# Optimization experiments

Hardware: AMD Instinct MI355X
Metric: run time of the kernel (lower is better)

Reference implementation:

```python
import jax, jax.numpy as jnp
import numpy as np

NS = [65536, 16384, 4096, 1024, 256, 64]          # nodes per level (64 = 8 graphs x 8 dense voxels)
ES = [1048576, 262144, 65536, 16384, 4096]        # edges per level (avg degree 16)
INS = [1, 15, 23, 31, 39]
OUTS = [12, 20, 28, 36, 44]
K = 5                                             # kernel_size


def setup_inputs():
    keys = iter(jax.random.split(jax.random.key(0), 64))
    d = {'x': jax.random.normal(next(keys), (NS[0], 1), jnp.float32),
         'pos': jax.random.uniform(next(keys), (NS[0], 3), jnp.float32)}
    for l in range(5):
        n, e, ci, co = NS[l], ES[l], INS[l], OUTS[l]
        d[f'src{l}'] = jax.random.randint(next(keys), (e,), 0, n)
        d[f'dst{l}'] = jax.random.randint(next(keys), (e,), 0, n)
        d[f'eattr{l}'] = jax.random.normal(next(keys), (e, 3), jnp.float32)
        d[f'cluster{l}'] = jax.random.randint(next(keys), (n,), 0, NS[l + 1])
        d[f'w1_{l}'] = jax.random.normal(next(keys), (3, K), jnp.float32) * 0.5
        d[f'b1_{l}'] = jnp.zeros((K,), jnp.float32)
        d[f'w2_{l}'] = jax.random.normal(next(keys), (K, ci * co), jnp.float32) / np.float32(np.sqrt(K * ci))
        d[f'b2_{l}'] = jnp.zeros((ci * co,), jnp.float32)
        d[f'root_{l}'] = jax.random.normal(next(keys), (ci, co), jnp.float32) / np.float32(np.sqrt(ci))
        d[f'bias_{l}'] = jnp.zeros((co,), jnp.float32)
    d['fc_w'] = jax.random.normal(next(keys), (8 * 47, 10), jnp.float32) / np.float32(np.sqrt(8 * 47))
    d['fc_b'] = jnp.zeros((10,), jnp.float32)
    return d


def _conv(x, src, dst, eattr, w1, b1, w2, b2, root, bias, n):
    # edge-conditioned kernel: MLP(edge_attr) -> [E, ci, co]
    h = jnp.tanh(eattr @ w1 + b1)                                  # [E, K]
    We = (h @ w2 + b2).reshape(eattr.shape[0], x.shape[1], -1)     # [E, ci, co]
    msg = jnp.einsum('ei,eio->eo', x[src], We)                     # gather + per-edge matvec
    s = jax.ops.segment_sum(msg, dst, num_segments=n)
    cnt = jax.ops.segment_sum(jnp.ones((dst.shape[0], 1), x.dtype), dst, num_segments=n)
    agg = s / jnp.maximum(cnt, 1.0)                                # mean aggregation
    return agg + x @ root + bias, jnp.mean(jnp.square(We))


def _pool(x, pos, cluster, n_next):
    # sparse voxel max pool on features, mean on positions; pos concatenated to features
    xm = jax.ops.segment_max(x, cluster, num_segments=n_next)
    xm = jnp.where(jnp.isfinite(xm), xm, 0.0)                      # empty voxels -> 0
    ps = jax.ops.segment_sum(pos, cluster, num_segments=n_next)
    cnt = jax.ops.segment_sum(jnp.ones((pos.shape[0], 1), pos.dtype), cluster, num_segments=n_next)
    pm = ps / jnp.maximum(cnt, 1.0)
    return jnp.concatenate([xm, pm], axis=1), pm


def reference(x, pos, src0, dst0, eattr0, cluster0, w1_0, b1_0, w2_0, b2_0, root_0, bias_0,
              src1, dst1, eattr1, cluster1, w1_1, b1_1, w2_1, b2_1, root_1, bias_1,
              src2, dst2, eattr2, cluster2, w1_2, b1_2, w2_2, b2_2, root_2, bias_2,
              src3, dst3, eattr3, cluster3, w1_3, b1_3, w2_3, b2_3, root_3, bias_3,
              src4, dst4, eattr4, cluster4, w1_4, b1_4, w2_4, b2_4, root_4, bias_4,
              fc_w, fc_b):
    lv = [(src0, dst0, eattr0, cluster0, w1_0, b1_0, w2_0, b2_0, root_0, bias_0),
          (src1, dst1, eattr1, cluster1, w1_1, b1_1, w2_1, b2_1, root_1, bias_1),
          (src2, dst2, eattr2, cluster2, w1_2, b1_2, w2_2, b2_2, root_2, bias_2),
          (src3, dst3, eattr3, cluster3, w1_3, b1_3, w2_3, b2_3, root_3, bias_3),
          (src4, dst4, eattr4, cluster4, w1_4, b1_4, w2_4, b2_4, root_4, bias_4)]
    closs = jnp.float32(0.0)
    for l, (src, dst, ea, cl, w1, b1, w2, b2, rt, bs) in enumerate(lv):
        x, c = _conv(x, src, dst, ea, w1, b1, w2, b2, rt, bs, NS[l])
        closs = closs + c
        x, pos = _pool(x, pos, cl, NS[l + 1])
    feat = x.reshape(-1, 8 * 47)                                   # [B, 8*47]
    logits = feat @ fc_w + fc_b
    return jax.nn.log_softmax(logits, axis=1), closs
```

## Files before the change

### kernel.cpp

```cpp
#include <hip/hip_runtime.h>
#include <hip/hip_fp16.h>
#include <math.h>


#define TILES0 1024
#define TSZ0   1024
#define NB0    512
#define TILES1 256
#define TSZ1   1024
#define NB1    512

__device__ __forceinline__ float ftanh(float x) {
    float e = __expf(2.f * x);
    return 1.f - 2.f / (e + 1.f);
}

struct SegArgs {
    const int* idx[10];
    int*       cnt[10];
    int*       rp [10];
    int*       out[10];
    int        n  [10];
    int        nb [10];
    int        tstart[11];
};

struct ScanAux {
    int* tilesum;
    int* tileoff;
    int  sstart[11];
    int  T;
};

struct HArgs {
    const float* eattr[5];
    const float* w1[5];
    const float* b1[5];
    float*       H;
    int          E[5];
    int          bstart[6];
};

struct WArgs {
    const float* w2[5];
    const float* b2[5];
    const float* H;
    float*       sq;
    int          cico[5];
    int          E[5];
};

__global__ __launch_bounds__(256) void countA_k(
    SegArgs a, HArgs ha, const int* __restrict__ dst0,
    const int* __restrict__ dst1, int* __restrict__ M, int* __restrict__ M1,
    int hsBlocks)
{
    __shared__ int sh[NB0];
    int B = blockIdx.x;
    int t = threadIdx.x;

    if (B < TILES0) {
        for (int u = t; u < NB0; u += 256) sh[u] = 0;
        __syncthreads();
        int base = B * TSZ0 + t;
        #pragma unroll
        for (int it = 0; it < 4; it++)
            atomicAdd(&sh[dst0[base + it * 256] >> 7], 1);
        __syncthreads();
        for (int u = t; u < NB0; u += 256) M[(size_t)B * NB0 + u] = sh[u];
        return;
    }
    B -= TILES0;
    if (B < TILES1) {
        for (int u = t; u < NB1; u += 256) sh[u] = 0;
        __syncthreads();
        int base = B * TSZ1 + t;
        #pragma unroll
        for (int it = 0; it < 4; it++)
            atomicAdd(&sh[dst1[base + it * 256] >> 5], 1);
        __syncthreads();
        for (int u = t; u < NB1; u += 256) M1[(size_t)B * NB1 + u] = sh[u];
        return;
    }
    B -= TILES1;
    if (B < hsBlocks) {
        const int K = 8;
        int l = 0;
        while (l < 4 && B >= ha.bstart[l + 1]) l++;
        int bloc = B - ha.bstart[l];
        const float* ea = ha.eattr[l];
        float w1r[15], b1r[5];
        #pragma unroll
        for (int i = 0; i < 15; i++) w1r[i] = ha.w1[l][i];
        #pragma unroll
        for (int i = 0; i < 5; i++)  b1r[i] = ha.b1[l][i];
        float acc[20];
        #pragma unroll
        for (int i = 0; i < 20; i++) acc[i] = 0.f;
        int base = bloc * 256 * K + t;
        for (int it = 0; it < K; it++) {
            int e = base + it * 256;
            if (e < ha.E[l]) {
                float e0 = ea[e * 3], e1 = ea[e * 3 + 1], e2 = ea[e * 3 + 2];
                float h[5];
                #pragma unroll
                for (int k = 0; k < 5; k++)
                    h[k] = ftanh(e0 * w1r[k] + e1 * w1r[5 + k] + e2 * w1r[10 + k] + b1r[k]);
                int p = 5;
                #pragma unroll
                for (int k = 0; k < 5; k++) {
                    acc[k] += h[k];
                    #pragma unroll
                    for (int k2 = k; k2 < 5; k2++) acc[p++] += h[k] * h[k2];
                }
            }
        }
        float* red = (float*)sh;
        int wid = t >> 6, lane = t & 63;
        #pragma unroll
        for (int v = 0; v < 20; v++) {
            float s = acc[v];
            #pragma unroll
            for (int o = 32; o; o >>= 1) s += __shfl_down(s, o);
            if (lane == 0) red[wid * 20 + v] = s;
        }
        __syncthreads();
        if (t < 20)
            atomicAdd(&ha.H[l * 20 + t],
                      red[t] + red[20 + t] + red[40 + t] + red[60 + t]);
        return;
    }
    B -= hsBlocks;
    {
        int s = 0;
        while (s < 9 && B >= a.tstart[s + 1]) s++;
        int i0 = (B - a.tstart[s]) * 1024;
        const int* idx = a.idx[s];
        int* cnt = a.cnt[s];
        int n = a.n[s];
        #pragma unroll
        for (int j = 0; j < 4; j++) {
            int i = i0 + j * 256 + t;
            if (i < n) atomicAdd(&cnt[idx[i]], 1);
        }
    }
}

__global__ __launch_bounds__(256) void scanP1_k(
    SegArgs a, ScanAux x, const int* __restrict__ M, int* __restrict__ M2,
    int* __restrict__ colTotal, const int* __restrict__ M1,
    int* __restrict__ M21, int* __restrict__ ct1)
{
    __shared__ int sc[256];
    int B = blockIdx.x;
    int t = threadIdx.x;

    if (B < NB0) {
        int v[4];
        int s4 = 0;
        #pragma unroll
        for (int j = 0; j < 4; j++) {
            v[j] = M[(size_t)(t * 4 + j) * NB0 + B];
            s4 += v[j];
        }
        sc[t] = s4;
        __syncthreads();
        for (int d = 1; d < 256; d <<= 1) {
            int u = (t >= d) ? sc[t - d] : 0;
            __syncthreads();
            sc[t] += u;
            __syncthreads();
        }
        int run = sc[t] - s4;
        #pragma unroll
        for (int j = 0; j < 4; j++) {
            M2[(size_t)(t * 4 + j) * NB0 + B] = run;
            run += v[j];
        }
        if (t == 255) colTotal[B] = sc[255];
        return;
    }
    B -= NB0;
    if (B < NB1) {
        int v = M1[(size_t)t * NB1 + B];
        sc[t] = v;
        __syncthreads();
        for (int d = 1; d < 256; d <<= 1) {
            int u = (t >= d) ? sc[t - d] : 0;
            __syncthreads();
            sc[t] += u;
            __syncthreads();
        }
        M21[(size_t)t * NB1 + B] = sc[t] - v;
        if (t == 255) ct1[B] = sc[255];
        return;
    }
    int b = B - NB1;
    int s = 0;
    while (s < 9 && b >= x.sstart[s + 1]) s++;
    int tloc = b - x.sstart[s];
    int nb = a.nb[s];
    const int* cnt = a.cnt[s];
    int i0 = tloc * 4096 + t * 16;
    int sum = 0;
    #pragma unroll
    for (int k = 0; k < 16; k++) {
        int i = i0 + k;
        if (i < nb) sum += cnt[i];
    }
    #pragma unroll
    for (int o = 32; o; o >>= 1) sum += __shfl_down(sum, o);
    if ((t & 63) == 0) sc[t >> 6] = sum;
    __syncthreads();
    if (t == 0)
        x.tilesum[b] = sc[0] + sc[1] + sc[2] + sc[3];
}

__global__ __launch_bounds__(512) void scanP2_k(
    SegArgs a, ScanAux x, const int* __restrict__ colTotal,
    int* __restrict__ bucketStart, const int* __restrict__ ct1,
    int* __restrict__ bs1)
{
    __shared__ int sc[NB0];
    int t = threadIdx.x;
    if (blockIdx.x == 0) {
        int v = colTotal[t];
        sc[t] = v;
        __syncthreads();
        for (int d = 1; d < NB0; d <<= 1) {
            int u = (t >= d) ? sc[t - d] : 0;
            __syncthreads();
            sc[t] += u;
            __syncthreads();
        }
        bucketStart[t] = sc[t] - v;
        if (t == NB0 - 1) bucketStart[NB0] = sc[NB0 - 1];
        return;
    }
    if (blockIdx.x == 2) {
        int v = ct1[t];
        sc[t] = v;
        __syncthreads();
        for (int d = 1; d < NB1; d <<= 1) {
            int u = (t >= d) ? sc[t - d] : 0;
            __syncthreads();
            sc[t] += u;
            __syncthreads();
        }
        bs1[t] = sc[t] - v;
        if (t == NB1 - 1) bs1[NB1] = sc[NB1 - 1];
        return;
    }
    if (t >= 64) return;
    int lane = t;
    int orig = (lane < x.T) ? x.tilesum[lane] : 0;
    int val = orig;
    #pragma unroll
    for (int d = 1; d < 64; d <<= 1) {
        int v = __shfl_up(val, d);
        if (lane >= d) val += v;
    }
    int excl = val - orig;
    int s = 0;
    while (s < 9 && lane >= x.sstart[s + 1]) s++;
    int segExcl = __shfl(excl, x.sstart[s]);
    if (lane < x.T) {
        x.tileoff[lane] = excl - segExcl;
        if (lane == x.sstart[s + 1] - 1)
            a.rp[s][a.nb[s]] = val - segExcl;
    }
}

__global__ __launch_bounds__(256) void scanP3_k(
    SegArgs a, ScanAux x,
    const int* __restrict__ src, const int* __restrict__ dst,
    const float* __restrict__ ea, const float* __restrict__ x0,
    const int* __restrict__ M2, const int* __restrict__ bucketStart,
    float4* __restrict__ pay2,
    const float* __restrict__ w1, const float* __restrict__ b1,
    float* __restrict__ H0,
    const int* __restrict__ src1, const int* __restrict__ dst1,
    const float* __restrict__ ea1, const int* __restrict__ M21,
    const int* __restrict__ bs1, float4* __restrict__ pay1)
{
    __shared__ int   shi[NB0];
    __shared__ float shf[100];
    int B = blockIdx.x;
    int t = threadIdx.x;

    if (B < TILES0) {
        int tile = B;
        for (int u = t; u < NB0; u += 256)
            shi[u] = bucketStart[u] + M2[(size_t)tile * NB0 + u];
        if (t < 15) shf[t] = w1[t];
        if (t >= 32 && t < 37) shf[15 + t - 32] = b1[t - 32];
        __syncthreads();

        float acc[20];
        #pragma unroll
        for (int i = 0; i < 20; i++) acc[i] = 0.f;

        int base = tile * TSZ0 + t;
        #pragma unroll
        for (int it = 0; it < 4; it++) {
            int i = base + it * 256;
            int d = dst[i];
            float e0 = ea[i * 3], e1 = ea[i * 3 + 1], e2 = ea[i * 3 + 2];
            float h[5];
            #pragma unroll
            for (int k = 0; k < 5; k++)
                h[k] = ftanh(e0 * shf[k] + e1 * shf[5 + k] + e2 * shf[10 + k] + shf[15 + k]);
            int p = 5;
            #pragma unroll
            for (int k = 0; k < 5; k++) {
                acc[k] += h[k];
                #pragma unroll
                for (int k2 = k; k2 < 5; k2++) acc[p++] += h[k] * h[k2];
            }
            float xv = x0[src[i]];
            union HU { __half2 h2; float f; } p01, p23;
            p01.h2 = __floats2half2_rn(h[0], h[1]);
            p23.h2 = __floats2half2_rn(h[2], h[3]);
            unsigned wbits = ((unsigned)d << 16) |
                             (unsigned)__half_as_ushort(__float2half_rn(h[4]));
            int ps = atomicAdd(&shi[d >> 7], 1);
            pay2[ps] = make_float4(xv, p01.f, p23.f, __uint_as_float(wbits));
        }

        int wid = t >> 6, lane = t & 63;
        #pragma unroll
        for (int v = 0; v < 20; v++) {
            float s = acc[v];
            #pragma unroll
            for (int o = 32; o; o >>= 1) s += __shfl_down(s, o);
            if (lane == 0) shf[20 + wid * 20 + v] = s;
        }
        __syncthreads();
        if (t < 20)
            atomicAdd(&H0[t], shf[20 + t] + shf[40 + t] + shf[60 + t] + shf[80 + t]);
        return;
    }
    B -= TILES0;
    if (B < TILES1) {
        int tile = B;
        for (int u = t; u < NB1; u += 256)
            shi[u] = bs1[u] + M21[(size_t)tile * NB1 + u];
        __syncthreads();
        int base = tile * TSZ1 + t;
        #pragma unroll
        for (int it = 0; it < 4; it++) {
            int i = base + it * 256;
            int d = dst1[i];
            int key = (d << 16) | src1[i];
            float e0 = ea1[i * 3], e1 = ea1[i * 3 + 1], e2 = ea1[i * 3 + 2];
            int ps = atomicAdd(&shi[d >> 5], 1);
            pay1[ps] = make_float4(__int_as_float(key), e0, e1, e2);
        }
        return;
    }
    B -= TILES1;
    int s = 0;
    while (s < 9 && B >= x.sstart[s + 1]) s++;
    int tloc = B - x.sstart[s];
    int nb = a.nb[s];
    const int* cnt = a.cnt[s];
    int* rp = a.rp[s];
    int i0 = tloc * 4096 + t * 16;
    int v[16];
    int sum = 0;
    #pragma unroll
    for (int k = 0; k < 16; k++) {
        int i = i0 + k;
        v[k] = (i < nb) ? cnt[i] : 0;
        sum += v[k];
    }
    int acc = sum;
    shi[t] = acc;
    __syncthreads();
    for (int d = 1; d < 256; d <<= 1) {
        int t2 = (t >= d) ? shi[t - d] : 0;
        __syncthreads();
        acc += t2;
        shi[t] = acc;
        __syncthreads();
    }
    int running = x.tileoff[B] + (acc - sum);
    #pragma unroll
    for (int k = 0; k < 16; k++) {
        int i = i0 + k;
        if (i < nb) rp[i] = running;
        running += v[k];
    }
}

__global__ __launch_bounds__(256) void scatC_k(
    SegArgs a, WArgs wa,
    const float4* __restrict__ pay2, const int* __restrict__ bucketStart,
    const float* __restrict__ w2, const float* __restrict__ b2,
    const float* __restrict__ root, const float* __restrict__ bias,
    const float* __restrict__ x, float* __restrict__ y,
    const float4* __restrict__ pay1, const int* __restrict__ bs1,
    int* __restrict__ rp1, float4* __restrict__ rec1)
{
    __shared__ float wsm[96];
    __shared__ float nacc[7 * 128];
    __shared__ int hist[32], st[32], cur[32];
    int B = blockIdx.x;
    int t = threadIdx.x;

    if (B < NB0) {
        if (t < 60) wsm[t] = w2[t];
        else if (t >= 64  && t < 76)  wsm[60 + t - 64]  = b2[t - 64];
        else if (t >= 128 && t < 140) wsm[72 + t - 128] = root[t - 128];
        else if (t >= 192 && t < 204) wsm[84 + t - 192] = bias[t - 192];
        for (int u = t; u < 7 * 128; u += 256) nacc[u] = 0.f;
        __syncthreads();

        int lo = bucketStart[B], hi = bucketStart[B + 1];
        int bin0 = B << 7;
        for (int j = lo + t; j < hi; j += 256) {
            float4 R = pay2[j];
            union HU { float f; __half2 h2; } a01, a23;
            a01.f = R.y; a23.f = R.z;
            unsigned wbits = __float_as_uint(R.w);
            int node = (int)(wbits >> 16) - bin0;
            float xv = R.x;
            atomicAdd(&nacc[node], xv);
            atomicAdd(&nacc[128 + node], __low2float(a01.h2)  * xv);
            atomicAdd(&nacc[256 + node], __high2float(a01.h2) * xv);
            atomicAdd(&nacc[384 + node], __low2float(a23.h2)  * xv);
            atomicAdd(&nacc[512 + node], __high2float(a23.h2) * xv);
            atomicAdd(&nacc[640 + node],
                      __half2float(__ushort_as_half((unsigned short)(wbits & 0xffffu))) * xv);
            atomicAdd(&nacc[768 + node], 1.f);
        }
        __syncthreads();

        if (t < 128) {
            int v = bin0 + t;
            float deg = nacc[768 + t];
            float S0 = nacc[t],       S1 = nacc[128 + t], S2 = nacc[256 + t];
            float S3 = nacc[384 + t], S4 = nacc[512 + t], S5 = nacc[640 + t];
            float inv = 1.f / fmaxf(deg, 1.f);
            float xv = x[v];
            #pragma unroll
            for (int o = 0; o < 12; o++) {
                float msg = wsm[60 + o] * S0 + wsm[o] * S1 + wsm[12 + o] * S2 +
                            wsm[24 + o] * S3 + wsm[36 + o] * S4 + wsm[48 + o] * S5;
                y[v * 12 + o] = msg * inv + xv * wsm[72 + o] + wsm[84 + o];
            }
        }
        return;
    }
    B -= NB0;
    if (B < NB1) {
        int b = B;
        int lo = bs1[b], hi = bs1[b + 1];
        int bin0 = b << 5;
        if (t < 32) hist[t] = 0;
        __syncthreads();
        const float* payw = (const float*)pay1;
        for (int j = lo + t; j < hi; j += 256) {
            int rel = (int)(__float_as_uint(payw[4 * j]) >> 16) - bin0;
            atomicAdd(&hist[rel], 1);
        }
        __syncthreads();
        if (t < 32) {
            int v = hist[t];
            int val = v;
            #pragma unroll
            for (int d = 1; d < 32; d <<= 1) {
                int u = __shfl_up(val, d);
                if (t >= d) val += u;
            }
            st[t] = val - v;
            cur[t] = lo + val - v;
            rp1[bin0 + t] = lo + val - v;
            if (b == NB1 - 1 && t == 31) rp1[NB1 * 32] = hi;
        }
        __syncthreads();
        for (int j = lo + t; j < hi; j += 256) {
            float4 R = pay1[j];
            int rel = (int)(__float_as_uint(R.x) >> 16) - bin0;
            int p = atomicAdd(&cur[rel], 1);
            rec1[p] = R;
        }
        return;
    }
    B -= NB1;
    if (B < 5) {
        if (t >= 64) return;
        int l = B;
        const float* w2l = wa.w2[l];
        const float* b2l = wa.b2[l];
        int cico = wa.cico[l];
        float d[21];
        #pragma unroll
        for (int i = 0; i < 21; i++) d[i] = 0.f;
        for (int u = t; u < cico; u += 64) {
            float b = b2l[u];
            float w[5];
            #pragma unroll
            for (int k = 0; k < 5; k++) w[k] = w2l[k * cico + u];
            int p = 0;
            #pragma unroll
            for (int k = 0; k < 5; k++) {
                #pragma unroll
                for (int k2 = k; k2 < 5; k2++) d[p++] += w[k] * w[k2];
            }
            #pragma unroll
            for (int k = 0; k < 5; k++) d[15 + k] += b * w[k];
            d[20] += b * b;
        }
        #pragma unroll
        for (int i = 0; i < 21; i++) {
            #pragma unroll
            for (int off = 32; off; off >>= 1) d[i] += __shfl_down(d[i], off);
        }
        if (t == 0) {
            const float* H1 = wa.H + l * 20;
            const float* H2 = H1 + 5;
            float sq = (float)wa.E[l] * d[20];
            #pragma unroll
            for (int k = 0; k < 5; k++) sq += 2.f * d[15 + k] * H1[k];
            int p = 0;
            #pragma unroll
            for (int k = 0; k < 5; k++) {
                #pragma unroll
                for (int k2 = k; k2 < 5; k2++) {
                    sq += ((k == k2) ? 1.f : 2.f) * d[p] * H2[p];
                    p++;
                }
            }
            wa.sq[l] = sq;
        }
        return;
    }
    B -= 5;
    {
        int s = 0;
        while (s < 9 && B >= a.tstart[s + 1]) s++;
        int i0 = (B - a.tstart[s]) * 1024;
        const int* idx = a.idx[s];
        int* cnt = a.cnt[s];
        const int* rp = a.rp[s];
        int* out = a.out[s];
        int n = a.n[s];
        #pragma unroll
        for (int j = 0; j < 4; j++) {
            int i = i0 + j * 256 + t;
            if (i < n) {
                int d = idx[i];
                int p = atomicSub(&cnt[d], 1) - 1;
                out[rp[d] + p] = i;
            }
        }
    }
}

__global__ __launch_bounds__(256) void conv1s_k(
    const int* __restrict__ rp, const float4* __restrict__ rec,
    const float* __restrict__ w1, const float* __restrict__ b1,
    const float* __restrict__ w2, const float* __restrict__ b2,
    const float* __restrict__ root, const float* __restrict__ bias,
    const float* __restrict__ x, float* __restrict__ y)
{
    constexpr int CI = 15, CO = 20, CH = 48, CICO = CI * CO;
    __shared__ float w1s[20];
    __shared__ float4 recb[CH];
    __shared__ int   svb[CH];
    __shared__ float hb[CH * 6];
    __shared__ float xs[CH * CI];
    __shared__ float S[6 * CI];

    int t = threadIdx.x;
    int v = blockIdx.x;
    if (t < 20) w1s[t] = (t < 15) ? w1[t] : b1[t - 15];
    int r0 = rp[v], r1 = rp[v + 1];
    int d  = r1 - r0;
    float acc = 0.f;

    for (int c0 = r0; c0 < r1; c0 += CH) {
        int cn = min(CH, r1 - c0);
        if (t < cn) {
            float4 R = rec[c0 + t];
            recb[t] = R;
            svb[t]  = (int)(__float_as_uint(R.x) & 0xffffu);
            hb[t * 6] = 1.f;
        }
        __syncthreads();
        if (t < cn * 5) {
            int j = t / 5, k = t % 5;
            float e0 = recb[j].y, e1 = recb[j].z, e2 = recb[j].w;
            hb[j * 6 + 1 + k] =
                ftanh(e0 * w1s[k] + e1 * w1s[5 + k] + e2 * w1s[10 + k] + w1s[15 + k]);
        }
        for (int u = t; u < cn * CI; u += 256)
            xs[u] = x[(size_t)svb[u / CI] * CI + (u % CI)];
        __syncthreads();
        if (t < 6 * CI) {
            int i = t / 6, k6 = t % 6;
            for (int j = 0; j < cn; j++)
                acc += hb[j * 6 + k6] * xs[j * CI + i];
        }
        __syncthreads();
    }

    if (t < 6 * CI) S[t] = acc;
    __syncthreads();

    if (t < CO) {
        float m = 0.f;
        for (int i = 0; i < CI; i++) {
            m += b2[i * CO + t] * S[i * 6];
            #pragma unroll
            for (int k = 0; k < 5; k++)
                m += w2[k * CICO + i * CO + t] * S[i * 6 + 1 + k];
        }
        m /= fmaxf((float)d, 1.f);
        for (int i = 0; i < CI; i++)
            m += x[(size_t)v * CI + i] * root[i * CO + t];
        y[(size_t)v * CO + t] = m + bias[t];
    }
}

template<int CI, int CO>
__global__ __launch_bounds__(256) void coop_conv_k(
    const int* __restrict__ rp, const int* __restrict__ eid,
    const int* __restrict__ src, const float* __restrict__ eattr,
    const float* __restrict__ w1, const float* __restrict__ b1,
    const float* __restrict__ w2, const float* __restrict__ b2,
    const float* __restrict__ root, const float* __restrict__ bias,
    const float* __restrict__ x, float* __restrict__ y)
{
    constexpr int CH   = 48;
    constexpr int CICO = CI * CO;
    __shared__ float w1s[20];
    __shared__ int   eb[CH], svb[CH];
    __shared__ float hb[CH * 6];
    __shared__ float xs[CH * CI];
    __shared__ float S[6 * CI];

    int t = threadIdx.x;
    int v = blockIdx.x;
    if (t < 20) w1s[t] = (t < 15) ? w1[t] : b1[t - 15];
    int r0 = rp[v], r1 = rp[v + 1];
    int d  = r1 - r0;
    float acc = 0.f;

    for (int c0 = r0; c0 < r1; c0 += CH) {
        int cn = min(CH, r1 - c0);
        if (t < cn) {
            int e = eid[c0 + t];
            eb[t]  = e;
            svb[t] = src[e];
            hb[t * 6] = 1.f;
        }
        __syncthreads();
        if (t < cn * 5) {
            int j = t / 5, k = t % 5;
            int e = eb[j];
            float e0 = eattr[e * 3], e1 = eattr[e * 3 + 1], e2 = eattr[e * 3 + 2];
            hb[j * 6 + 1 + k] =
                ftanh(e0 * w1s[k] + e1 * w1s[5 + k] + e2 * w1s[10 + k] + w1s[15 + k]);
        }
        for (int u = t; u < cn * CI; u += 256)
            xs[u] = x[(size_t)svb[u / CI] * CI + (u % CI)];
        __syncthreads();
        if (t < 6 * CI) {
            int i = t / 6, k6 = t % 6;
            for (int j = 0; j < cn; j++)
                acc += hb[j * 6 + k6] * xs[j * CI + i];
        }
        __syncthreads();
    }

    if (t < 6 * CI) S[t] = acc;
    __syncthreads();

    if (t < CO) {
        float m = 0.f;
        for (int i = 0; i < CI; i++) {
            m += b2[i * CO + t] * S[i * 6];
            #pragma unroll
            for (int k = 0; k < 5; k++)
                m += w2[k * CICO + i * CO + t] * S[i * 6 + 1 + k];
        }
        m /= fmaxf((float)d, 1.f);
        for (int i = 0; i < CI; i++)
            m += x[(size_t)v * CI + i] * root[i * CO + t];
        y[(size_t)v * CO + t] = m + bias[t];
    }
}

template<int CO>
__global__ __launch_bounds__(256) void pool_k(
    int NN,
    const int* __restrict__ crp, const int* __restrict__ cnid,
    const float* __restrict__ y, const float* __restrict__ pos,
    float* __restrict__ xn, float* __restrict__ pn)
{
    int t = blockIdx.x * 256 + threadIdx.x;
    if (t >= NN * (CO + 3)) return;
    int c = t / (CO + 3), o = t % (CO + 3);
    int r0 = crp[c], r1 = crp[c + 1];
    int d = r1 - r0;
    if (o < CO) {
        float m = -INFINITY;
        for (int j = r0; j < r1; j++)
            m = fmaxf(m, y[(size_t)cnid[j] * CO + o]);
        if (d == 0 || !isfinite(m)) m = 0.f;
        xn[c * (CO + 3) + o] = m;
    } else {
        int k = o - CO;
        float sum = 0.f;
        for (int j = r0; j < r1; j++)
            sum += pos[cnid[j] * 3 + k];
        float pm = sum / fmaxf((float)d, 1.f);
        xn[c * (CO + 3) + CO + k] = pm;
        pn[c * 3 + k] = pm;
    }
}

__global__ __launch_bounds__(128) void fc_k(
    const float* __restrict__ x5,
    const float* __restrict__ fc_w, const float* __restrict__ fc_b,
    const float* __restrict__ sq, float* __restrict__ out)
{
    __shared__ float feat[8 * 376];
    __shared__ float logit[80];
    __shared__ float roff[8];
    for (int t = threadIdx.x; t < 8 * 376; t += 128) feat[t] = x5[t];
    __syncthreads();
    int t = threadIdx.x;
    if (t < 80) {
        int b = t / 10, j = t % 10;
        float acc = fc_b[j];
        for (int k = 0; k < 376; k++) acc += feat[b * 376 + k] * fc_w[k * 10 + j];
        logit[t] = acc;
    }
    __syncthreads();
    if (t < 8) {
        float m = -1e30f;
        for (int j = 0; j < 10; j++) m = fmaxf(m, logit[t * 10 + j]);
        float ssum = 0.f;
        for (int j = 0; j < 10; j++) ssum += expf(logit[t * 10 + j] - m);
        roff[t] = m + logf(ssum);
    }
    __syncthreads();
    if (t < 80) out[t] = logit[t] - roff[t / 10];
    if (t == 0) {
        float closs = 0.f;
        closs += sq[0] * (1.0f / 12582912.0f);
        closs += sq[1] * (1.0f / 78643200.0f);
        closs += sq[2] * (1.0f / 42205184.0f);
        closs += sq[3] * (1.0f / 18284544.0f);
        closs += sq[4] * (1.0f / 7028736.0f);
        out[80] = closs;
    }
}


extern "C" void kernel_launch(void* const* d_in, const int* in_sizes, int n_in,
                              void* d_out, int out_size, void* d_ws, size_t ws_size,
                              hipStream_t stream)
{
    static const int NSa[6] = {65536, 16384, 4096, 1024, 256, 64};
    static const int ESa[5] = {1048576, 262144, 65536, 16384, 4096};
    static const int COa[5] = {12, 20, 28, 36, 44};
    static const int CIa[5] = {1, 15, 23, 31, 39};

    const float* x0   = (const float*)d_in[0];
    const float* pos0 = (const float*)d_in[1];

    int* wsw = (int*)d_ws;
    size_t off = 0;
    auto alw = [&](size_t n) -> size_t {
        size_t p = off; off += (n + 63) & ~(size_t)63; return p;
    };
    size_t degO[5], cdegO[5];
    for (int l = 2; l < 5; l++) degO[l]  = alw(NSa[l]);
    for (int l = 0; l < 5; l++) cdegO[l] = alw(NSa[l + 1]);
    size_t HO = alw(100);
    size_t zeroWords = off;
    size_t rpO[5], crpO[5], eidO[5], cnidO[5];
    rpO[1] = alw(NSa[1] + 1);
    for (int l = 2; l < 5; l++) rpO[l]  = alw(NSa[l] + 1);
    for (int l = 0; l < 5; l++) crpO[l] = alw(NSa[l + 1] + 1);
    for (int l = 2; l < 5; l++) eidO[l] = alw(ESa[l]);
    for (int l = 0; l < 5; l++) cnidO[l] = alw(NSa[l]);
    size_t tsO  = alw(64);
    size_t toO  = alw(64);
    size_t MO   = alw((size_t)TILES0 * NB0);
    size_t M2O  = alw((size_t)TILES0 * NB0);
    size_t ctO  = alw(NB0);
    size_t bsO  = alw(NB0 + 1);
    size_t payO = alw((size_t)ESa[0] * 4);
    size_t M1O  = alw((size_t)TILES1 * NB1);
    size_t M21O = alw((size_t)TILES1 * NB1);
    size_t ct1O = alw(NB1);
    size_t bs1O = alw(NB1 + 1);
    size_t pay1O = alw((size_t)ESa[1] * 4);
    size_t rec1O = alw((size_t)ESa[1] * 4);
    size_t yO   = alw((size_t)65536 * 12);
    size_t sqO  = alw(8);
    size_t xnO[5], pnO[5];
    for (int l = 0; l < 5; l++) xnO[l] = alw((size_t)NSa[l + 1] * (COa[l] + 3));
    for (int l = 0; l < 5; l++) pnO[l] = alw((size_t)NSa[l] * 3 / 4 + 64);
    for (int l = 0; l < 5; l++) pnO[l] = alw((size_t)NSa[l + 1] * 3);

    hipMemsetAsync(d_ws, 0, zeroWords * 4, stream);

    SegArgs sa{};
    int nseg = 0;
    for (int l = 2; l < 5; l++) {
        sa.idx[nseg] = (const int*)d_in[3 + 10 * l];
        sa.cnt[nseg] = wsw + degO[l];
        sa.rp [nseg] = wsw + rpO[l];
        sa.out[nseg] = wsw + eidO[l];
        sa.n  [nseg] = ESa[l];
        sa.nb [nseg] = NSa[l];
        nseg++;
    }
    for (int l = 0; l < 5; l++) {
        sa.idx[nseg] = (const int*)d_in[5 + 10 * l];
        sa.cnt[nseg] = wsw + cdegO[l];
        sa.rp [nseg] = wsw + crpO[l];
        sa.out[nseg] = wsw + cnidO[l];
        sa.n  [nseg] = NSa[l];
        sa.nb [nseg] = NSa[l + 1];
        nseg++;
    }
    ScanAux sx{};
    int tiles = 0, btiles = 0;
    for (int s = 0; s < nseg; s++) {
        sa.tstart[s] = tiles;
        tiles += (sa.n[s] + 1023) / 1024;
        sx.sstart[s] = btiles;
        btiles += (sa.nb[s] + 4095) / 4096;
    }
    for (int s = nseg; s <= 10; s++) {
        sa.tstart[s] = tiles;
        sx.sstart[s] = btiles;
        if (s < 10) {
            sa.idx[s] = sa.idx[nseg - 1]; sa.cnt[s] = sa.cnt[nseg - 1];
            sa.rp[s] = sa.rp[nseg - 1];   sa.out[s] = sa.out[nseg - 1];
            sa.n[s] = 0; sa.nb[s] = 8;
        }
    }
    sx.T = btiles;
    sx.tilesum = wsw + tsO;
    sx.tileoff = wsw + toO;

    float4* pay2 = (float4*)(wsw + payO);
    float4* pay1 = (float4*)(wsw + pay1O);
    float4* rec1 = (float4*)(wsw + rec1O);
    float*  Hp   = (float*)(wsw + HO);

    HArgs ha{};
    int bs = 0;
    ha.bstart[0] = 0;
    ha.eattr[0] = (const float*)d_in[4];
    ha.w1[0] = (const float*)d_in[6];
    ha.b1[0] = (const float*)d_in[7];
    ha.E[0] = 0;
    for (int l = 1; l < 5; l++) {
        ha.eattr[l] = (const float*)d_in[4 + 10 * l];
        ha.w1[l]    = (const float*)d_in[6 + 10 * l];
        ha.b1[l]    = (const float*)d_in[7 + 10 * l];
        ha.E[l]     = ESa[l];
        ha.bstart[l] = bs;
        bs += (ESa[l] + 2047) / 2048;
    }
    ha.bstart[5] = bs;
    ha.H = Hp;

    WArgs wa{};
    for (int l = 0; l < 5; l++) {
        wa.w2[l]   = (const float*)d_in[8 + 10 * l];
        wa.b2[l]   = (const float*)d_in[9 + 10 * l];
        wa.cico[l] = CIa[l] * COa[l];
        wa.E[l]    = ESa[l];
    }
    wa.H  = Hp;
    wa.sq = (float*)(wsw + sqO);

    countA_k<<<TILES0 + TILES1 + bs + tiles, 256, 0, stream>>>(
        sa, ha, (const int*)d_in[3], (const int*)d_in[13],
        wsw + MO, wsw + M1O, bs);
    scanP1_k<<<NB0 + NB1 + btiles, 256, 0, stream>>>(
        sa, sx, wsw + MO, wsw + M2O, wsw + ctO,
        wsw + M1O, wsw + M21O, wsw + ct1O);
    scanP2_k<<<3, 512, 0, stream>>>(sa, sx, wsw + ctO, wsw + bsO,
                                    wsw + ct1O, wsw + bs1O);
    scanP3_k<<<TILES0 + TILES1 + btiles, 256, 0, stream>>>(
        sa, sx,
        (const int*)d_in[2], (const int*)d_in[3], (const float*)d_in[4],
        x0, wsw + M2O, wsw + bsO, pay2,
        (const float*)d_in[6], (const float*)d_in[7], Hp,
        (const int*)d_in[12], (const int*)d_in[13], (const float*)d_in[14],
        wsw + M21O, wsw + bs1O, pay1);

    float* yb = (float*)(wsw + yO);

    scatC_k<<<NB0 + NB1 + 5 + tiles, 256, 0, stream>>>(
        sa, wa, pay2, wsw + bsO,
        (const float*)d_in[8], (const float*)d_in[9],
        (const float*)d_in[10], (const float*)d_in[11], x0, yb,
        pay1, wsw + bs1O, wsw + rpO[1], rec1);

    pool_k<12><<<(NSa[1] * 15 + 255) / 256, 256, 0, stream>>>(
        NSa[1], wsw + crpO[0], wsw + cnidO[0], yb, pos0,
        (float*)(wsw + xnO[0]), (float*)(wsw + pnO[0]));

    conv1s_k<<<NSa[1], 256, 0, stream>>>(
        wsw + rpO[1], rec1,
        (const float*)d_in[16], (const float*)d_in[17],
        (const float*)d_in[18], (const float*)d_in[19],
        (const float*)d_in[20], (const float*)d_in[21],
        (const float*)(wsw + xnO[0]), yb);
    pool_k<20><<<(NSa[2] * 23 + 255) / 256, 256, 0, stream>>>(
        NSa[2], wsw + crpO[1], wsw + cnidO[1], yb,
        (const float*)(wsw + pnO[0]),
        (float*)(wsw + xnO[1]), (float*)(wsw + pnO[1]));

#define LVLC(l, CI_, CO_) do {                                                 \
    const float* xin   = (const float*)(wsw + xnO[(l) - 1]);                   \
    const float* posin = (const float*)(wsw + pnO[(l) - 1]);                   \
    int N = NSa[(l)], NN = NSa[(l) + 1];                                       \
    coop_conv_k<CI_, CO_><<<N, 256, 0, stream>>>(                              \
        wsw + rpO[(l)], wsw + eidO[(l)],                                       \
        (const int*)d_in[2 + 10 * (l)], (const float*)d_in[4 + 10 * (l)],      \
        (const float*)d_in[6 + 10 * (l)], (const float*)d_in[7 + 10 * (l)],    \
        (const float*)d_in[8 + 10 * (l)], (const float*)d_in[9 + 10 * (l)],    \
        (const float*)d_in[10 + 10 * (l)], (const float*)d_in[11 + 10 * (l)],  \
        xin, yb);                                                              \
    pool_k<CO_><<<(NN * ((CO_) + 3) + 255) / 256, 256, 0, stream>>>(           \
        NN, wsw + crpO[(l)], wsw + cnidO[(l)], yb, posin,                      \
        (float*)(wsw + xnO[(l)]), (float*)(wsw + pnO[(l)]));                   \
} while (0)

    LVLC(2, 23, 28);
    LVLC(3, 31, 36);
    LVLC(4, 39, 44);
#undef LVLC

    fc_k<<<1, 128, 0, stream>>>((const float*)(wsw + xnO[4]),
                                (const float*)d_in[52], (const float*)d_in[53],
                                wa.sq, (float*)d_out);
}
```

Measured before the change: 403.6 us.

## Fuse all stages into one persistent cooperative kernel with grid syncs

Replaces the sequence of separate kernel launches (count, scan phases, scatter, per-level conv and pool, fc) with a single persistent cooperative kernel. A fixed grid of 1024 blocks loops over each stage's virtual blocks and separates stages with grid.sync(). If the cooperative launch fails, it falls back to launching one kernel per stage. This is meant to remove launch overhead and the idle tails between the many small dependent kernels. In exchange, every stage runs under a fixed block count with shared-memory and register limits set for the whole kernel, which can lower per-stage efficiency.

```diff
diff --git a/kernel.cpp b/kernel.cpp
--- a/kernel.cpp
+++ b/kernel.cpp
@@ -1,6 +1,9 @@
 #include <hip/hip_runtime.h>
 #include <hip/hip_fp16.h>
+#include <hip/hip_cooperative_groups.h>
 #include <math.h>
+
+namespace cg = cooperative_groups;
 
 
 #define TILES0 1024
@@ -50,659 +53,69 @@
     int          E[5];
 };
 
-__global__ __launch_bounds__(256) void countA_k(
-    SegArgs a, HArgs ha, const int* __restrict__ dst0,
-    const int* __restrict__ dst1, int* __restrict__ M, int* __restrict__ M1,
-    int hsBlocks)
+struct MegaArgs {
+    SegArgs sa; ScanAux sx; HArgs ha; WArgs wa;
+    const int* src0; const int* dst0; const float* ea0;
+    const int* src1; const int* dst1; const float* ea1;
+    const float* x0; const float* pos0;
+    int* M; int* M2; int* colTotal; int* bucketStart;
+    int* M1; int* M21; int* ct1; int* bs1;
+    float4* pay2; float4* pay1; float4* rec1; int* rp1;
+    const float* w1[5]; const float* b1[5]; const float* w2[5]; const float* b2[5];
+    const float* root[5]; const float* bias[5];
+    const int* rp[5]; const int* eid[5]; const int* srcL[5]; const float* eaL[5];
+    const int* crp[5]; const int* cnid[5];
+    float* y; float* xn[5]; float* pn[5];
+    const float* fc_w; const float* fc_b; float* out;
+    int hsB;
+    int W[16];
+};
+
+
+__device__ void scan512(const int* __restrict__ in, int* __restrict__ outExcl,
+                        int t, int* sc)
 {
-    __shared__ int sh[NB0];
-    int B = blockIdx.x;
-    int t = threadIdx.x;
-
-    if (B < TILES0) {
-        for (int u = t; u < NB0; u += 256) sh[u] = 0;
-        __syncthreads();
-        int base = B * TSZ0 + t;
-        #pragma unroll
-        for (int it = 0; it < 4; it++)
-            atomicAdd(&sh[dst0[base + it * 256] >> 7], 1);
-        __syncthreads();
-        for (int u = t; u < NB0; u += 256) M[(size_t)B * NB0 + u] = sh[u];
-        return;
-    }
-    B -= TILES0;
-    if (B < TILES1) {
-        for (int u = t; u < NB1; u += 256) sh[u] = 0;
-        __syncthreads();
-        int base = B * TSZ1 + t;
-        #pragma unroll
-        for (int it = 0; it < 4; it++)
-            atomicAdd(&sh[dst1[base + it * 256] >> 5], 1);
-        __syncthreads();
-        for (int u = t; u < NB1; u += 256) M1[(size_t)B * NB1 + u] = sh[u];
-        return;
-    }
-    B -= TILES1;
-    if (B < hsBlocks) {
-        const int K = 8;
-        int l = 0;
-        while (l < 4 && B >= ha.bstart[l + 1]) l++;
-        int bloc = B - ha.bstart[l];
-        const float* ea = ha.eattr[l];
-        float w1r[15], b1r[5];
-        #pragma unroll
-        for (int i = 0; i < 15; i++) w1r[i] = ha.w1[l][i];
-        #pragma unroll
-        for (int i = 0; i < 5; i++)  b1r[i] = ha.b1[l][i];
-        float acc[20];
-        #pragma unroll
-        for (int i = 0; i < 20; i++) acc[i] = 0.f;
-        int base = bloc * 256 * K + t;
-        for (int it = 0; it < K; it++) {
-            int e = base + it * 256;
-            if (e < ha.E[l]) {
-                float e0 = ea[e * 3], e1 = ea[e * 3 + 1], e2 = ea[e * 3 + 2];
-                float h[5];
-                #pragma unroll
-                for (int k = 0; k < 5; k++)
-                    h[k] = ftanh(e0 * w1r[k] + e1 * w1r[5 + k] + e2 * w1r[10 + k] + b1r[k]);
-                int p = 5;
-                #pragma unroll
-                for (int k = 0; k < 5; k++) {
-                    acc[k] += h[k];
-                    #pragma unroll
-                    for (int k2 = k; k2 < 5; k2++) acc[p++] += h[k] * h[k2];
-                }
-            }
-        }
-        float* red = (float*)sh;
-        int wid = t >> 6, lane = t & 63;
-        #pragma unroll
-        for (int v = 0; v < 20; v++) {
-            float s = acc[v];
-            #pragma unroll
-            for (int o = 32; o; o >>= 1) s += __shfl_down(s, o);
-            if (lane == 0) red[wid * 20 + v] = s;
-        }
-        __syncthreads();
-        if (t < 20)
-            atomicAdd(&ha.H[l * 20 + t],
-                      red[t] + red[20 + t] + red[40 + t] + red[60 + t]);
-        return;
-    }
-    B -= hsBlocks;
-    {
-        int s = 0;
-        while (s < 9 && B >= a.tstart[s + 1]) s++;
-        int i0 = (B - a.tstart[s]) * 1024;
-        const int* idx = a.idx[s];
-        int* cnt = a.cnt[s];
-        int n = a.n[s];
-        #pragma unroll
-        for (int j = 0; j < 4; j++) {
-            int i = i0 + j * 256 + t;
-            if (i < n) atomicAdd(&cnt[idx[i]], 1);
-        }
-    }
-}
-
-__global__ __launch_bounds__(256) void scanP1_k(
-    SegArgs a, ScanAux x, const int* __restrict__ M, int* __restrict__ M2,
-    int* __restrict__ colTotal, const int* __restrict__ M1,
-    int* __restrict__ M21, int* __restrict__ ct1)
-{
-    __shared__ int sc[256];
-    int B = blockIdx.x;
-    int t = threadIdx.x;
-
-    if (B < NB0) {
-        int v[4];
-        int s4 = 0;
-        #pragma unroll
-        for (int j = 0; j < 4; j++) {
-            v[j] = M[(size_t)(t * 4 + j) * NB0 + B];
-            s4 += v[j];
-        }
-        sc[t] = s4;
-        __syncthreads();
-        for (int d = 1; d < 256; d <<= 1) {
-            int u = (t >= d) ? sc[t - d] : 0;
-            __syncthreads();
-            sc[t] += u;
-            __syncthreads();
-        }
-        int run = sc[t] - s4;
-        #pragma unroll
-        for (int j = 0; j < 4; j++) {
-            M2[(size_t)(t * 4 + j) * NB0 + B] = run;
-            run += v[j];
-        }
-        if (t == 255) colTotal[B] = sc[255];
-        return;
-    }
-    B -= NB0;
-    if (B < NB1) {
-        int v = M1[(size_t)t * NB1 + B];
-        sc[t] = v;
-        __syncthreads();
-        for (int d = 1; d < 256; d <<= 1) {
-            int u = (t >= d) ? sc[t - d] : 0;
-            __syncthreads();
-            sc[t] += u;
-            __syncthreads();
-        }
-        M21[(size_t)t * NB1 + B] = sc[t] - v;
-        if (t == 255) ct1[B] = sc[255];
-        return;
-    }
-    int b = B - NB1;
-    int s = 0;
-    while (s < 9 && b >= x.sstart[s + 1]) s++;
-    int tloc = b - x.sstart[s];
-    int nb = a.nb[s];
-    const int* cnt = a.cnt[s];
-    int i0 = tloc * 4096 + t * 16;
-    int sum = 0;
-    #pragma unroll
-    for (int k = 0; k < 16; k++) {
-        int i = i0 + k;
-        if (i < nb) sum += cnt[i];
-    }
-    #pragma unroll
-    for (int o = 32; o; o >>= 1) sum += __shfl_down(sum, o);
-    if ((t & 63) == 0) sc[t >> 6] = sum;
-    __syncthreads();
-    if (t == 0)
-        x.tilesum[b] = sc[0] + sc[1] + sc[2] + sc[3];
-}
-
-__global__ __launch_bounds__(512) void scanP2_k(
-    SegArgs a, ScanAux x, const int* __restrict__ colTotal,
-    int* __restrict__ bucketStart, const int* __restrict__ ct1,
-    int* __restrict__ bs1)
-{
-    __shared__ int sc[NB0];
-    int t = threadIdx.x;
-    if (blockIdx.x == 0) {
-        int v = colTotal[t];
-        sc[t] = v;
-        __syncthreads();
-        for (int d = 1; d < NB0; d <<= 1) {
-            int u = (t >= d) ? sc[t - d] : 0;
-            __syncthreads();
-            sc[t] += u;
-            __syncthreads();
-        }
-        bucketStart[t] = sc[t] - v;
-        if (t == NB0 - 1) bucketStart[NB0] = sc[NB0 - 1];
-        return;
-    }
-    if (blockIdx.x == 2) {
-        int v = ct1[t];
-        sc[t] = v;
-        __syncthreads();
-        for (int d = 1; d < NB1; d <<= 1) {
-            int u = (t >= d) ? sc[t - d] : 0;
-            __syncthreads();
-            sc[t] += u;
-            __syncthreads();
-        }
-        bs1[t] = sc[t] - v;
-        if (t == NB1 - 1) bs1[NB1] = sc[NB1 - 1];
-        return;
-    }
-    if (t >= 64) return;
-    int lane = t;
-    int orig = (lane < x.T) ? x.tilesum[lane] : 0;
-    int val = orig;
-    #pragma unroll
-    for (int d = 1; d < 64; d <<= 1) {
-        int v = __shfl_up(val, d);
-        if (lane >= d) val += v;
-    }
-    int excl = val - orig;
-    int s = 0;
-    while (s < 9 && lane >= x.sstart[s + 1]) s++;
-    int segExcl = __shfl(excl, x.sstart[s]);
-    if (lane < x.T) {
-        x.tileoff[lane] = excl - segExcl;
-        if (lane == x.sstart[s + 1] - 1)
-            a.rp[s][a.nb[s]] = val - segExcl;
-    }
-}
-
-__global__ __launch_bounds__(256) void scanP3_k(
-    SegArgs a, ScanAux x,
-    const int* __restrict__ src, const int* __restrict__ dst,
-    const float* __restrict__ ea, const float* __restrict__ x0,
-    const int* __restrict__ M2, const int* __restrict__ bucketStart,
-    float4* __restrict__ pay2,
-    const float* __restrict__ w1, const float* __restrict__ b1,
-    float* __restrict__ H0,
-    const int* __restrict__ src1, const int* __restrict__ dst1,
-    const float* __restrict__ ea1, const int* __restrict__ M21,
-    const int* __restrict__ bs1, float4* __restrict__ pay1)
-{
-    __shared__ int   shi[NB0];
-    __shared__ float shf[100];
-    int B = blockIdx.x;
-    int t = threadIdx.x;
-
-    if (B < TILES0) {
-        int tile = B;
-        for (int u = t; u < NB0; u += 256)
-            shi[u] = bucketStart[u] + M2[(size_t)tile * NB0 + u];
-        if (t < 15) shf[t] = w1[t];
-        if (t >= 32 && t < 37) shf[15 + t - 32] = b1[t - 32];
-        __syncthreads();
-
-        float acc[20];
-        #pragma unroll
-        for (int i = 0; i < 20; i++) acc[i] = 0.f;
-
-        int base = tile * TSZ0 + t;
-        #pragma unroll
-        for (int it = 0; it < 4; it++) {
-            int i = base + it * 256;
-            int d = dst[i];
-            float e0 = ea[i * 3], e1 = ea[i * 3 + 1], e2 = ea[i * 3 + 2];
-            float h[5];
-            #pragma unroll
-            for (int k = 0; k < 5; k++)
-                h[k] = ftanh(e0 * shf[k] + e1 * shf[5 + k] + e2 * shf[10 + k] + shf[15 + k]);
-            int p = 5;
-            #pragma unroll
-            for (int k = 0; k < 5; k++) {
-                acc[k] += h[k];
-                #pragma unroll
-                for (int k2 = k; k2 < 5; k2++) acc[p++] += h[k] * h[k2];
-            }
-            float xv = x0[src[i]];
-            union HU { __half2 h2; float f; } p01, p23;
-            p01.h2 = __floats2half2_rn(h[0], h[1]);
-            p23.h2 = __floats2half2_rn(h[2], h[3]);
-            unsigned wbits = ((unsigned)d << 16) |
-                             (unsigned)__half_as_ushort(__float2half_rn(h[4]));
-            int ps = atomicAdd(&shi[d >> 7], 1);
-            pay2[ps] = make_float4(xv, p01.f, p23.f, __uint_as_float(wbits));
-        }
-
-        int wid = t >> 6, lane = t & 63;
-        #pragma unroll
-        for (int v = 0; v < 20; v++) {
-            float s = acc[v];
-            #pragma unroll
-            for (int o = 32; o; o >>= 1) s += __shfl_down(s, o);
-            if (lane == 0) shf[20 + wid * 20 + v] = s;
-        }
-        __syncthreads();
-        if (t < 20)
-            atomicAdd(&H0[t], shf[20 + t] + shf[40 + t] + shf[60 + t] + shf[80 + t]);
-        return;
-    }
-    B -= TILES0;
-    if (B < TILES1) {
-        int tile = B;
-        for (int u = t; u < NB1; u += 256)
-            shi[u] = bs1[u] + M21[(size_t)tile * NB1 + u];
-        __syncthreads();
-        int base = tile * TSZ1 + t;
-        #pragma unroll
-        for (int it = 0; it < 4; it++) {
-            int i = base + it * 256;
-            int d = dst1[i];
-            int key = (d << 16) | src1[i];
-            float e0 = ea1[i * 3], e1 = ea1[i * 3 + 1], e2 = ea1[i * 3 + 2];
-            int ps = atomicAdd(&shi[d >> 5], 1);
-            pay1[ps] = make_float4(__int_as_float(key), e0, e1, e2);
-        }
-        return;
-    }
-    B -= TILES1;
-    int s = 0;
-    while (s < 9 && B >= x.sstart[s + 1]) s++;
-    int tloc = B - x.sstart[s];
-    int nb = a.nb[s];
-    const int* cnt = a.cnt[s];
-    int* rp = a.rp[s];
-    int i0 = tloc * 4096 + t * 16;
-    int v[16];
-    int sum = 0;
-    #pragma unroll
-    for (int k = 0; k < 16; k++) {
-        int i = i0 + k;
-        v[k] = (i < nb) ? cnt[i] : 0;
-        sum += v[k];
-    }
-    int acc = sum;
-    shi[t] = acc;
+    int a0 = in[2 * t], a1 = in[2 * t + 1];
+    int ps = a0 + a1;
+    sc[t] = ps;
     __syncthreads();
     for (int d = 1; d < 256; d <<= 1) {
-        int t2 = (t >= d) ? shi[t - d] : 0;
+        int u = (t >= d) ? sc[t - d] : 0;
         __syncthreads();
-        acc += t2;
-        shi[t] = acc;
+        sc[t] += u;
         __syncthreads();
     }
-    int running = x.tileoff[B] + (acc - sum);
-    #pragma unroll
-    for (int k = 0; k < 16; k++) {
-        int i = i0 + k;
-        if (i < nb) rp[i] = running;
-        running += v[k];
-    }
+    int excl = sc[t] - ps;
+    outExcl[2 * t]     = excl;
+    outExcl[2 * t + 1] = excl + a0;
+    if (t == 255) outExcl[512] = sc[255];
 }
 
-__global__ __launch_bounds__(256) void scatC_k(
-    SegArgs a, WArgs wa,
-    const float4* __restrict__ pay2, const int* __restrict__ bucketStart,
-    const float* __restrict__ w2, const float* __restrict__ b2,
-    const float* __restrict__ root, const float* __restrict__ bias,
-    const float* __restrict__ x, float* __restrict__ y,
-    const float4* __restrict__ pay1, const int* __restrict__ bs1,
-    int* __restrict__ rp1, float4* __restrict__ rec1)
+__device__ __forceinline__ void c0_accum(float* nacc, int bin0, float4 R)
 {
-    __shared__ float wsm[96];
-    __shared__ float nacc[7 * 128];
-    __shared__ int hist[32], st[32], cur[32];
-    int B = blockIdx.x;
-    int t = threadIdx.x;
-
-    if (B < NB0) {
-        if (t < 60) wsm[t] = w2[t];
-        else if (t >= 64  && t < 76)  wsm[60 + t - 64]  = b2[t - 64];
-        else if (t >= 128 && t < 140) wsm[72 + t - 128] = root[t - 128];
-        else if (t >= 192 && t < 204) wsm[84 + t - 192] = bias[t - 192];
-        for (int u = t; u < 7 * 128; u += 256) nacc[u] = 0.f;
-        __syncthreads();
-
-        int lo = bucketStart[B], hi = bucketStart[B + 1];
-        int bin0 = B << 7;
-        for (int j = lo + t; j < hi; j += 256) {
-            float4 R = pay2[j];
-            union HU { float f; __half2 h2; } a01, a23;
-            a01.f = R.y; a23.f = R.z;
-            unsigned wbits = __float_as_uint(R.w);
-            int node = (int)(wbits >> 16) - bin0;
-            float xv = R.x;
-            atomicAdd(&nacc[node], xv);
-            atomicAdd(&nacc[128 + node], __low2float(a01.h2)  * xv);
-            atomicAdd(&nacc[256 + node], __high2float(a01.h2) * xv);
-            atomicAdd(&nacc[384 + node], __low2float(a23.h2)  * xv);
-            atomicAdd(&nacc[512 + node], __high2float(a23.h2) * xv);
-            atomicAdd(&nacc[640 + node],
-                      __half2float(__ushort_as_half((unsigned short)(wbits & 0xffffu))) * xv);
-            atomicAdd(&nacc[768 + node], 1.f);
-        }
-        __syncthreads();
-
-        if (t < 128) {
-            int v = bin0 + t;
-            float deg = nacc[768 + t];
-            float S0 = nacc[t],       S1 = nacc[128 + t], S2 = nacc[256 + t];
-            float S3 = nacc[384 + t], S4 = nacc[512 + t], S5 = nacc[640 + t];
-            float inv = 1.f / fmaxf(deg, 1.f);
-            float xv = x[v];
-            #pragma unroll
-            for (int o = 0; o < 12; o++) {
-                float msg = wsm[60 + o] * S0 + wsm[o] * S1 + wsm[12 + o] * S2 +
-                            wsm[24 + o] * S3 + wsm[36 + o] * S4 + wsm[48 + o] * S5;
-                y[v * 12 + o] = msg * inv + xv * wsm[72 + o] + wsm[84 + o];
-            }
-        }
-        return;
-    }
-    B -= NB0;
-    if (B < NB1) {
-        int b = B;
-        int lo = bs1[b], hi = bs1[b + 1];
-        int bin0 = b << 5;
-        if (t < 32) hist[t] = 0;
-        __syncthreads();
-        const float* payw = (const float*)pay1;
-        for (int j = lo + t; j < hi; j += 256) {
-            int rel = (int)(__float_as_uint(payw[4 * j]) >> 16) - bin0;
-            atomicAdd(&hist[rel], 1);
-        }
-        __syncthreads();
-        if (t < 32) {
-            int v = hist[t];
-            int val = v;
-            #pragma unroll
-            for (int d = 1; d < 32; d <<= 1) {
-                int u = __shfl_up(val, d);
-                if (t >= d) val += u;
-            }
-            st[t] = val - v;
-            cur[t] = lo + val - v;
-            rp1[bin0 + t] = lo + val - v;
-            if (b == NB1 - 1 && t == 31) rp1[NB1 * 32] = hi;
-        }
-        __syncthreads();
-        for (int j = lo + t; j < hi; j += 256) {
-            float4 R = pay1[j];
-            int rel = (int)(__float_as_uint(R.x) >> 16) - bin0;
-            int p = atomicAdd(&cur[rel], 1);
-            rec1[p] = R;
-        }
-        return;
-    }
-    B -= NB1;
-    if (B < 5) {
-        if (t >= 64) return;
-        int l = B;
-        const float* w2l = wa.w2[l];
-        const float* b2l = wa.b2[l];
-        int cico = wa.cico[l];
-        float d[21];
-        #pragma unroll
-        for (int i = 0; i < 21; i++) d[i] = 0.f;
-        for (int u = t; u < cico; u += 64) {
-            float b = b2l[u];
-            float w[5];
-            #pragma unroll
-            for (int k = 0; k < 5; k++) w[k] = w2l[k * cico + u];
-            int p = 0;
-            #pragma unroll
-            for (int k = 0; k < 5; k++) {
-                #pragma unroll
-                for (int k2 = k; k2 < 5; k2++) d[p++] += w[k] * w[k2];
-            }
-            #pragma unroll
-            for (int k = 0; k < 5; k++) d[15 + k] += b * w[k];
-            d[20] += b * b;
-        }
-        #pragma unroll
-        for (int i = 0; i < 21; i++) {
-            #pragma unroll
-            for (int off = 32; off; off >>= 1) d[i] += __shfl_down(d[i], off);
-        }
-        if (t == 0) {
-            const float* H1 = wa.H + l * 20;
-            const float* H2 = H1 + 5;
-            float sq = (float)wa.E[l] * d[20];
-            #pragma unroll
-            for (int k = 0; k < 5; k++) sq += 2.f * d[15 + k] * H1[k];
-            int p = 0;
-            #pragma unroll
-            for (int k = 0; k < 5; k++) {
-                #pragma unroll
-                for (int k2 = k; k2 < 5; k2++) {
-                    sq += ((k == k2) ? 1.f : 2.f) * d[p] * H2[p];
-                    p++;
-                }
-            }
-            wa.sq[l] = sq;
-        }
-        return;
-    }
-    B -= 5;
-    {
-        int s = 0;
-        while (s < 9 && B >= a.tstart[s + 1]) s++;
-        int i0 = (B - a.tstart[s]) * 1024;
-        const int* idx = a.idx[s];
-        int* cnt = a.cnt[s];
-        const int* rp = a.rp[s];
-        int* out = a.out[s];
-        int n = a.n[s];
-        #pragma unroll
-        for (int j = 0; j < 4; j++) {
-            int i = i0 + j * 256 + t;
-            if (i < n) {
-                int d = idx[i];
-                int p = atomicSub(&cnt[d], 1) - 1;
-                out[rp[d] + p] = i;
-            }
-        }
-    }
+    union HU { float f; __half2 h2; } a01, a23;
+    a01.f = R.y; a23.f = R.z;
+    unsigned wbits = __float_as_uint(R.w);
+    int node = (int)(wbits >> 16) - bin0;
+    float xv = R.x;
+    atomicAdd(&nacc[node], xv);
+    atomicAdd(&nacc[128 + node], __low2float(a01.h2)  * xv);
+    atomicAdd(&nacc[256 + node], __high2float(a01.h2) * xv);
+    atomicAdd(&nacc[384 + node], __low2float(a23.h2)  * xv);
+    atomicAdd(&nacc[512 + node], __high2float(a23.h2) * xv);
+    atomicAdd(&nacc[640 + node],
+              __half2float(__ushort_as_half((unsigned short)(wbits & 0xffffu))) * xv);
+    atomicAdd(&nacc[768 + node], 1.f);
 }
 
-__global__ __launch_bounds__(256) void conv1s_k(
-    const int* __restrict__ rp, const float4* __restrict__ rec,
-    const float* __restrict__ w1, const float* __restrict__ b1,
-    const float* __restrict__ w2, const float* __restrict__ b2,
-    const float* __restrict__ root, const float* __restrict__ bias,
-    const float* __restrict__ x, float* __restrict__ y)
+template<int CO>
+__device__ void pool_body(int NN, const int* __restrict__ crp,
+                          const int* __restrict__ cnid,
+                          const float* __restrict__ y, const float* __restrict__ pos,
+                          float* __restrict__ xn, float* __restrict__ pn, int gt)
 {
-    constexpr int CI = 15, CO = 20, CH = 48, CICO = CI * CO;
-    __shared__ float w1s[20];
-    __shared__ float4 recb[CH];
-    __shared__ int   svb[CH];
-    __shared__ float hb[CH * 6];
-    __shared__ float xs[CH * CI];
-    __shared__ float S[6 * CI];
-
-    int t = threadIdx.x;
-    int v = blockIdx.x;
-    if (t < 20) w1s[t] = (t < 15) ? w1[t] : b1[t - 15];
-    int r0 = rp[v], r1 = rp[v + 1];
-    int d  = r1 - r0;
-    float acc = 0.f;
-
-    for (int c0 = r0; c0 < r1; c0 += CH) {
-        int cn = min(CH, r1 - c0);
-        if (t < cn) {
-            float4 R = rec[c0 + t];
-            recb[t] = R;
-            svb[t]  = (int)(__float_as_uint(R.x) & 0xffffu);
-            hb[t * 6] = 1.f;
-        }
-        __syncthreads();
-        if (t < cn * 5) {
-            int j = t / 5, k = t % 5;
-            float e0 = recb[j].y, e1 = recb[j].z, e2 = recb[j].w;
-            hb[j * 6 + 1 + k] =
-                ftanh(e0 * w1s[k] + e1 * w1s[5 + k] + e2 * w1s[10 + k] + w1s[15 + k]);
-        }
-        for (int u = t; u < cn * CI; u += 256)
-            xs[u] = x[(size_t)svb[u / CI] * CI + (u % CI)];
-        __syncthreads();
-        if (t < 6 * CI) {
-            int i = t / 6, k6 = t % 6;
-            for (int j = 0; j < cn; j++)
-                acc += hb[j * 6 + k6] * xs[j * CI + i];
-        }
-        __syncthreads();
-    }
-
-    if (t < 6 * CI) S[t] = acc;
-    __syncthreads();
-
-    if (t < CO) {
-        float m = 0.f;
-        for (int i = 0; i < CI; i++) {
-            m += b2[i * CO + t] * S[i * 6];
-            #pragma unroll
-            for (int k = 0; k < 5; k++)
-                m += w2[k * CICO + i * CO + t] * S[i * 6 + 1 + k];
-        }
-        m /= fmaxf((float)d, 1.f);
-        for (int i = 0; i < CI; i++)
-            m += x[(size_t)v * CI + i] * root[i * CO + t];
-        y[(size_t)v * CO + t] = m + bias[t];
-    }
-}
-
-template<int CI, int CO>
-__global__ __launch_bounds__(256) void coop_conv_k(
-    const int* __restrict__ rp, const int* __restrict__ eid,
-    const int* __restrict__ src, const float* __restrict__ eattr,
-    const float* __restrict__ w1, const float* __restrict__ b1,
-    const float* __restrict__ w2, const float* __restrict__ b2,
-    const float* __restrict__ root, const float* __restrict__ bias,
-    const float* __restrict__ x, float* __restrict__ y)
-{
-    constexpr int CH   = 48;
-    constexpr int CICO = CI * CO;
-    __shared__ float w1s[20];
-    __shared__ int   eb[CH], svb[CH];
-    __shared__ float hb[CH * 6];
-    __shared__ float xs[CH * CI];
-    __shared__ float S[6 * CI];
-
-    int t = threadIdx.x;
-    int v = blockIdx.x;
-    if (t < 20) w1s[t] = (t < 15) ? w1[t] : b1[t - 15];
-    int r0 = rp[v], r1 = rp[v + 1];
-    int d  = r1 - r0;
-    float acc = 0.f;
-
-    for (int c0 = r0; c0 < r1; c0 += CH) {
-        int cn = min(CH, r1 - c0);
-        if (t < cn) {
-            int e = eid[c0 + t];
-            eb[t]  = e;
-            svb[t] = src[e];
-            hb[t * 6] = 1.f;
-        }
-        __syncthreads();
-        if (t < cn * 5) {
-            int j = t / 5, k = t % 5;
-            int e = eb[j];
-            float e0 = eattr[e * 3], e1 = eattr[e * 3 + 1], e2 = eattr[e * 3 + 2];
-            hb[j * 6 + 1 + k] =
-                ftanh(e0 * w1s[k] + e1 * w1s[5 + k] + e2 * w1s[10 + k] + w1s[15 + k]);
-        }
-        for (int u = t; u < cn * CI; u += 256)
-            xs[u] = x[(size_t)svb[u / CI] * CI + (u % CI)];
-        __syncthreads();
-        if (t < 6 * CI) {
-            int i = t / 6, k6 = t % 6;
-            for (int j = 0; j < cn; j++)
-                acc += hb[j * 6 + k6] * xs[j * CI + i];
-        }
-        __syncthreads();
-    }
-
-    if (t < 6 * CI) S[t] = acc;
-    __syncthreads();
-
-    if (t < CO) {
-        float m = 0.f;
-        for (int i = 0; i < CI; i++) {
-            m += b2[i * CO + t] * S[i * 6];
-            #pragma unroll
-            for (int k = 0; k < 5; k++)
-                m += w2[k * CICO + i * CO + t] * S[i * 6 + 1 + k];
-        }
-        m /= fmaxf((float)d, 1.f);
-        for (int i = 0; i < CI; i++)
-            m += x[(size_t)v * CI + i] * root[i * CO + t];
-        y[(size_t)v * CO + t] = m + bias[t];
-    }
-}
-
-template<int CO>
-__global__ __launch_bounds__(256) void pool_k(
-    int NN,
-    const int* __restrict__ crp, const int* __restrict__ cnid,
-    const float* __restrict__ y, const float* __restrict__ pos,
-    float* __restrict__ xn, float* __restrict__ pn)
-{
-    int t = blockIdx.x * 256 + threadIdx.x;
-    if (t >= NN * (CO + 3)) return;
-    int c = t / (CO + 3), o = t % (CO + 3);
+    if (gt >= NN * (CO + 3)) return;
+    int c = gt / (CO + 3), o = gt % (CO + 3);
     int r0 = crp[c], r1 = crp[c + 1];
     int d = r1 - r0;
     if (o < CO) {
@@ -722,42 +135,706 @@
     }
 }
 
-__global__ __launch_bounds__(128) void fc_k(
-    const float* __restrict__ x5,
-    const float* __restrict__ fc_w, const float* __restrict__ fc_b,
-    const float* __restrict__ sq, float* __restrict__ out)
+template<int CI, int CO>
+__device__ void coop_body(const MegaArgs& A, int l, int v, int t,
+                          float* SP, int* iSP)
 {
-    __shared__ float feat[8 * 376];
-    __shared__ float logit[80];
-    __shared__ float roff[8];
-    for (int t = threadIdx.x; t < 8 * 376; t += 128) feat[t] = x5[t];
+    constexpr int CH = 48, CICO = CI * CO;
+    int*   eb  = iSP;
+    int*   svb = iSP + 48;
+    float* w1s = SP + 96;
+    float* hb  = SP + 116;
+    float* Sx  = SP + 404;
+    float* xs  = SP + 640;
+    const int* rp = A.rp[l]; const int* eid = A.eid[l];
+    const int* src = A.srcL[l]; const float* eattr = A.eaL[l];
+    const float* x = A.xn[l - 1]; float* y = A.y;
+
+    if (t < 20) w1s[t] = (t < 15) ? A.w1[l][t] : A.b1[l][t - 15];
+    int r0 = rp[v], r1 = rp[v + 1];
+    int d = r1 - r0;
+    float acc = 0.f;
+
+    for (int c0 = r0; c0 < r1; c0 += CH) {
+        int cn = min(CH, r1 - c0);
+        if (t < cn) {
+            int e = eid[c0 + t];
+            eb[t]  = e;
+            svb[t] = src[e];
+            hb[t * 6] = 1.f;
+        }
+        __syncthreads();
+        if (t < cn * 5) {
+            int j = t / 5, k = t % 5;
+            int e = eb[j];
+            float e0 = eattr[e * 3], e1 = eattr[e * 3 + 1], e2 = eattr[e * 3 + 2];
+            hb[j * 6 + 1 + k] =
+                ftanh(e0 * w1s[k] + e1 * w1s[5 + k] + e2 * w1s[10 + k] + w1s[15 + k]);
+        }
+        for (int u = t; u < cn * CI; u += 256)
+            xs[u] = x[(size_t)svb[u / CI] * CI + (u % CI)];
+        __syncthreads();
+        if (t < 6 * CI) {
+            int i = t / 6, k6 = t % 6;
+            for (int j = 0; j < cn; j++)
+                acc += hb[j * 6 + k6] * xs[j * CI + i];
+        }
+        __syncthreads();
+    }
+
+    if (t < 6 * CI) Sx[t] = acc;
     __syncthreads();
-    int t = threadIdx.x;
-    if (t < 80) {
-        int b = t / 10, j = t % 10;
-        float acc = fc_b[j];
-        for (int k = 0; k < 376; k++) acc += feat[b * 376 + k] * fc_w[k * 10 + j];
-        logit[t] = acc;
+
+    if (t < CO) {
+        float m = 0.f;
+        const float* w2 = A.w2[l]; const float* b2 = A.b2[l];
+        for (int i = 0; i < CI; i++) {
+            m += b2[i * CO + t] * Sx[i * 6];
+            #pragma unroll
+            for (int k = 0; k < 5; k++)
+                m += w2[k * CICO + i * CO + t] * Sx[i * 6 + 1 + k];
+        }
+        m /= fmaxf((float)d, 1.f);
+        for (int i = 0; i < CI; i++)
+            m += x[(size_t)v * CI + i] * A.root[l][i * CO + t];
+        y[(size_t)v * CO + t] = m + A.bias[l][t];
     }
     __syncthreads();
-    if (t < 8) {
-        float m = -1e30f;
-        for (int j = 0; j < 10; j++) m = fmaxf(m, logit[t * 10 + j]);
-        float ssum = 0.f;
-        for (int j = 0; j < 10; j++) ssum += expf(logit[t * 10 + j] - m);
-        roff[t] = m + logf(ssum);
-    }
+}
+
+__device__ void conv1s_body(const MegaArgs& A, int v, int t, float* SP, int* iSP)
+{
+    constexpr int CI = 15, CO = 20, CH = 48, CICO = CI * CO;
+    float4* recb = (float4*)SP;
+    int*    svb  = iSP + 192;
+    float*  hb   = SP + 240;
+    float*  xs   = SP + 528;
+    float*  Sx   = SP + 1248;
+    float*  w1s  = SP + 1344;
+    const float* x = A.xn[0]; float* y = A.y;
+
+    if (t < 20) w1s[t] = (t < 15) ? A.w1[1][t] : A.b1[1][t - 15];
+    int r0 = A.rp1[v], r1 = A.rp1[v + 1];
+    int d = r1 - r0;
+    float acc = 0.f;
+
+    for (int c0 = r0; c0 < r1; c0 += CH) {
+        int cn = min(CH, r1 - c0);
+        if (t < cn) {
+            float4 R = A.rec1[c0 + t];
+            recb[t] = R;
+            svb[t]  = (int)(__float_as_uint(R.x) & 0xffffu);
+            hb[t * 6] = 1.f;
+        }
+        __syncthreads();
+        if (t < cn * 5) {
+            int j = t / 5, k = t % 5;
+            float e0 = recb[j].y, e1 = recb[j].z, e2 = recb[j].w;
+            hb[j * 6 + 1 + k] =
+                ftanh(e0 * w1s[k] + e1 * w1s[5 + k] + e2 * w1s[10 + k] + w1s[15 + k]);
+        }
+        for (int u = t; u < cn * CI; u += 256)
+            xs[u] = x[(size_t)svb[u / CI] * CI + (u % CI)];
+        __syncthreads();
+        if (t < 6 * CI) {
+            int i = t / 6, k6 = t % 6;
+            for (int j = 0; j < cn; j++)
+                acc += hb[j * 6 + k6] * xs[j * CI + i];
+        }
+        __syncthreads();
+    }
+
+    if (t < 6 * CI) Sx[t] = acc;
     __syncthreads();
-    if (t < 80) out[t] = logit[t] - roff[t / 10];
-    if (t == 0) {
-        float closs = 0.f;
-        closs += sq[0] * (1.0f / 12582912.0f);
-        closs += sq[1] * (1.0f / 78643200.0f);
-        closs += sq[2] * (1.0f / 42205184.0f);
-        closs += sq[3] * (1.0f / 18284544.0f);
-        closs += sq[4] * (1.0f / 7028736.0f);
-        out[80] = closs;
-    }
+
+    if (t < CO) {
+        float m = 0.f;
+        const float* w2 = A.w2[1]; const float* b2 = A.b2[1];
+        for (int i = 0; i < CI; i++) {
+            m += b2[i * CO + t] * Sx[i * 6];
+            #pragma unroll
+            for (int k = 0; k < 5; k++)
+                m += w2[k * CICO + i * CO + t] * Sx[i * 6 + 1 + k];
+        }
+        m /= fmaxf((float)d, 1.f);
+        for (int i = 0; i < CI; i++)
+            m += x[(size_t)v * CI + i] * A.root[1][i * CO + t];
+        y[(size_t)v * CO + t] = m + A.bias[1][t];
+    }
+    __syncthreads();
+}
+
+__device__ void run_stage(const MegaArgs& A, int s, int vb, int t, float* SP)
+{
+    int* iSP = (int*)SP;
+
+    switch (s) {
+    case 1: {
+        int B = vb;
+        if (B < TILES0) {
+            int* sh = iSP;
+            for (int u = t; u < NB0; u += 256) sh[u] = 0;
+            __syncthreads();
+            int base = B * TSZ0 + t;
+            #pragma unroll
+            for (int it = 0; it < 4; it++)
+                atomicAdd(&sh[A.dst0[base + it * 256] >> 7], 1);
+            __syncthreads();
+            for (int u = t; u < NB0; u += 256) A.M[(size_t)B * NB0 + u] = sh[u];
+            break;
+        }
+        B -= TILES0;
+        if (B < TILES1) {
+            int* sh = iSP;
+            for (int u = t; u < NB1; u += 256) sh[u] = 0;
+            __syncthreads();
+            int base = B * TSZ1 + t;
+            #pragma unroll
+            for (int it = 0; it < 4; it++)
+                atomicAdd(&sh[A.dst1[base + it * 256] >> 5], 1);
+            __syncthreads();
+            for (int u = t; u < NB1; u += 256) A.M1[(size_t)B * NB1 + u] = sh[u];
+            break;
+        }
+        B -= TILES1;
+        if (B < A.hsB) {
+            const HArgs& ha = A.ha;
+            const int K = 8;
+            int l = 0;
+            while (l < 4 && B >= ha.bstart[l + 1]) l++;
+            int bloc = B - ha.bstart[l];
+            const float* ea = ha.eattr[l];
+            float w1r[15], b1r[5];
+            #pragma unroll
+            for (int i = 0; i < 15; i++) w1r[i] = ha.w1[l][i];
+            #pragma unroll
+            for (int i = 0; i < 5; i++)  b1r[i] = ha.b1[l][i];
+            float acc[20];
+            #pragma unroll
+            for (int i = 0; i < 20; i++) acc[i] = 0.f;
+            int base = bloc * 256 * K + t;
+            for (int it = 0; it < K; it++) {
+                int e = base + it * 256;
+                if (e < ha.E[l]) {
+                    float e0 = ea[e * 3], e1 = ea[e * 3 + 1], e2 = ea[e * 3 + 2];
+                    float h[5];
+                    #pragma unroll
+                    for (int k = 0; k < 5; k++)
+                        h[k] = ftanh(e0 * w1r[k] + e1 * w1r[5 + k] + e2 * w1r[10 + k] + b1r[k]);
+                    int p = 5;
+                    #pragma unroll
+                    for (int k = 0; k < 5; k++) {
+                        acc[k] += h[k];
+                        #pragma unroll
+                        for (int k2 = k; k2 < 5; k2++) acc[p++] += h[k] * h[k2];
+                    }
+                }
+            }
+            float* red = SP;
+            int wid = t >> 6, lane = t & 63;
+            #pragma unroll
+            for (int v = 0; v < 20; v++) {
+                float sv = acc[v];
+                #pragma unroll
+                for (int o = 32; o; o >>= 1) sv += __shfl_down(sv, o);
+                if (lane == 0) red[wid * 20 + v] = sv;
+            }
+            __syncthreads();
+            if (t < 20)
+                atomicAdd(&ha.H[l * 20 + t],
+                          red[t] + red[20 + t] + red[40 + t] + red[60 + t]);
+            break;
+        }
+        B -= A.hsB;
+        {
+            const SegArgs& a = A.sa;
+            int sg = 0;
+            while (sg < 9 && B >= a.tstart[sg + 1]) sg++;
+            int i0 = (B - a.tstart[sg]) * 1024;
+            const int* idx = a.idx[sg];
+            int* cnt = a.cnt[sg];
+            int n = a.n[sg];
+            #pragma unroll
+            for (int j = 0; j < 4; j++) {
+                int i = i0 + j * 256 + t;
+                if (i < n) atomicAdd(&cnt[idx[i]], 1);
+            }
+        }
+        break;
+    }
+
+    case 2: {
+        int B = vb;
+        int* sc = iSP;
+        if (B < NB0) {
+            int v[4];
+            int s4 = 0;
+            #pragma unroll
+            for (int j = 0; j < 4; j++) {
+                v[j] = A.M[(size_t)(t * 4 + j) * NB0 + B];
+                s4 += v[j];
+            }
+            sc[t] = s4;
+            __syncthreads();
+            for (int d = 1; d < 256; d <<= 1) {
+                int u = (t >= d) ? sc[t - d] : 0;
+                __syncthreads();
+                sc[t] += u;
+                __syncthreads();
+            }
+            int run = sc[t] - s4;
+            #pragma unroll
+            for (int j = 0; j < 4; j++) {
+                A.M2[(size_t)(t * 4 + j) * NB0 + B] = run;
+                run += v[j];
+            }
+            if (t == 255) A.colTotal[B] = sc[255];
+            break;
+        }
+        B -= NB0;
+        if (B < NB1) {
+            int v = A.M1[(size_t)t * NB1 + B];
+            sc[t] = v;
+            __syncthreads();
+            for (int d = 1; d < 256; d <<= 1) {
+                int u = (t >= d) ? sc[t - d] : 0;
+                __syncthreads();
+                sc[t] += u;
+                __syncthreads();
+            }
+            A.M21[(size_t)t * NB1 + B] = sc[t] - v;
+            if (t == 255) A.ct1[B] = sc[255];
+            break;
+        }
+        {
+            int b = B - NB1;
+            const SegArgs& a = A.sa;
+            const ScanAux& x = A.sx;
+            int sg = 0;
+            while (sg < 9 && b >= x.sstart[sg + 1]) sg++;
+            int tloc = b - x.sstart[sg];
+            int nb = a.nb[sg];
+            const int* cnt = a.cnt[sg];
+            int i0 = tloc * 4096 + t * 16;
+            int sum = 0;
+            #pragma unroll
+            for (int k = 0; k < 16; k++) {
+                int i = i0 + k;
+                if (i < nb) sum += cnt[i];
+            }
+            #pragma unroll
+            for (int o = 32; o; o >>= 1) sum += __shfl_down(sum, o);
+            if ((t & 63) == 0) sc[t >> 6] = sum;
+            __syncthreads();
+            if (t == 0)
+                x.tilesum[b] = sc[0] + sc[1] + sc[2] + sc[3];
+        }
+        break;
+    }
+
+    case 3: {
+        if (vb == 0) {
+            scan512(A.colTotal, A.bucketStart, t, iSP);
+        } else if (vb == 2) {
+            scan512(A.ct1, A.bs1, t, iSP);
+        } else if (t < 64) {
+            const SegArgs& a = A.sa;
+            const ScanAux& x = A.sx;
+            int lane = t;
+            int orig = (lane < x.T) ? x.tilesum[lane] : 0;
+            int val = orig;
+            #pragma unroll
+            for (int d = 1; d < 64; d <<= 1) {
+                int v = __shfl_up(val, d);
+                if (lane >= d) val += v;
+            }
+            int excl = val - orig;
+            int sg = 0;
+            while (sg < 9 && lane >= x.sstart[sg + 1]) sg++;
+            int segExcl = __shfl(excl, x.sstart[sg]);
+            if (lane < x.T) {
+                x.tileoff[lane] = excl - segExcl;
+                if (lane == x.sstart[sg + 1] - 1)
+                    a.rp[sg][a.nb[sg]] = val - segExcl;
+            }
+        }
+        break;
+    }
+
+    case 4: {
+        int B = vb;
+        if (B < TILES0) {
+            int* shi = iSP;
+            float* shf = SP + 512;
+            int tile = B;
+            for (int u = t; u < NB0; u += 256)
+                shi[u] = A.bucketStart[u] + A.M2[(size_t)tile * NB0 + u];
+            if (t < 15) shf[t] = A.w1[0][t];
+            if (t >= 32 && t < 37) shf[15 + t - 32] = A.b1[0][t - 32];
+            __syncthreads();
+
+            float acc[20];
+            #pragma unroll
+            for (int i = 0; i < 20; i++) acc[i] = 0.f;
+
+            int base = tile * TSZ0 + t;
+            #pragma unroll
+            for (int it = 0; it < 4; it++) {
+                int i = base + it * 256;
+                int d = A.dst0[i];
+                float e0 = A.ea0[i * 3], e1 = A.ea0[i * 3 + 1], e2 = A.ea0[i * 3 + 2];
+                float h[5];
+                #pragma unroll
+                for (int k = 0; k < 5; k++)
+                    h[k] = ftanh(e0 * shf[k] + e1 * shf[5 + k] + e2 * shf[10 + k] + shf[15 + k]);
+                int p = 5;
+                #pragma unroll
+                for (int k = 0; k < 5; k++) {
+                    acc[k] += h[k];
+                    #pragma unroll
+                    for (int k2 = k; k2 < 5; k2++) acc[p++] += h[k] * h[k2];
+                }
+                float xv = A.x0[A.src0[i]];
+                union HU { __half2 h2; float f; } p01, p23;
+                p01.h2 = __floats2half2_rn(h[0], h[1]);
+                p23.h2 = __floats2half2_rn(h[2], h[3]);
+                unsigned wbits = ((unsigned)d << 16) |
+                                 (unsigned)__half_as_ushort(__float2half_rn(h[4]));
+                int ps = atomicAdd(&shi[d >> 7], 1);
+                A.pay2[ps] = make_float4(xv, p01.f, p23.f, __uint_as_float(wbits));
+            }
+
+            int wid = t >> 6, lane = t & 63;
+            #pragma unroll
+            for (int v = 0; v < 20; v++) {
+                float sv = acc[v];
+                #pragma unroll
+                for (int o = 32; o; o >>= 1) sv += __shfl_down(sv, o);
+                if (lane == 0) shf[20 + wid * 20 + v] = sv;
+            }
+            __syncthreads();
+            if (t < 20)
+                atomicAdd(&A.ha.H[t],
+                          shf[20 + t] + shf[40 + t] + shf[60 + t] + shf[80 + t]);
+            break;
+        }
+        B -= TILES0;
+        if (B < TILES1) {
+            int* shi = iSP;
+            int tile = B;
+            for (int u = t; u < NB1; u += 256)
+                shi[u] = A.bs1[u] + A.M21[(size_t)tile * NB1 + u];
+            __syncthreads();
+            int base = tile * TSZ1 + t;
+            #pragma unroll
+            for (int it = 0; it < 4; it++) {
+                int i = base + it * 256;
+                int d = A.dst1[i];
+                int key = (d << 16) | A.src1[i];
+                float e0 = A.ea1[i * 3], e1 = A.ea1[i * 3 + 1], e2 = A.ea1[i * 3 + 2];
+                int ps = atomicAdd(&shi[d >> 5], 1);
+                A.pay1[ps] = make_float4(__int_as_float(key), e0, e1, e2);
+            }
+            break;
+        }
+        {
+            int b = B - TILES1;
+            const SegArgs& a = A.sa;
+            const ScanAux& x = A.sx;
+            int* shi = iSP;
+            int sg = 0;
+            while (sg < 9 && b >= x.sstart[sg + 1]) sg++;
+            int tloc = b - x.sstart[sg];
+            int nb = a.nb[sg];
+            const int* cnt = a.cnt[sg];
+            int* rp = a.rp[sg];
+            int i0 = tloc * 4096 + t * 16;
+            int v[16];
+            int sum = 0;
+            #pragma unroll
+            for (int k = 0; k < 16; k++) {
+                int i = i0 + k;
+                v[k] = (i < nb) ? cnt[i] : 0;
+                sum += v[k];
+            }
+            int acc = sum;
+            shi[t] = acc;
+            __syncthreads();
+            for (int d = 1; d < 256; d <<= 1) {
+                int t2 = (t >= d) ? shi[t - d] : 0;
+                __syncthreads();
+                acc += t2;
+                shi[t] = acc;
+                __syncthreads();
+            }
+            int running = x.tileoff[b] + (acc - sum);
+            #pragma unroll
+            for (int k = 0; k < 16; k++) {
+                int i = i0 + k;
+                if (i < nb) rp[i] = running;
+                running += v[k];
+            }
+        }
+        break;
+    }
+
+    case 5: {
+        int B = vb;
+        if (B < NB0) {
+            float* wsm  = SP;
+            float* nacc = SP + 96;
+            if (t < 60) wsm[t] = A.w2[0][t];
+            else if (t >= 64  && t < 76)  wsm[60 + t - 64]  = A.b2[0][t - 64];
+            else if (t >= 128 && t < 140) wsm[72 + t - 128] = A.root[0][t - 128];
+            else if (t >= 192 && t < 204) wsm[84 + t - 192] = A.bias[0][t - 192];
+            for (int u = t; u < 7 * 128; u += 256) nacc[u] = 0.f;
+            __syncthreads();
+
+            int lo = A.bucketStart[B], hi = A.bucketStart[B + 1];
+            int bin0 = B << 7;
+            for (int j0 = lo + t; j0 < hi; j0 += 1024) {
+                float4 R0 = A.pay2[j0];
+                float4 R1, R2, R3;
+                bool g1 = j0 + 256 < hi, g2 = j0 + 512 < hi, g3 = j0 + 768 < hi;
+                if (g1) R1 = A.pay2[j0 + 256];
+                if (g2) R2 = A.pay2[j0 + 512];
+                if (g3) R3 = A.pay2[j0 + 768];
+                c0_accum(nacc, bin0, R0);
+                if (g1) c0_accum(nacc, bin0, R1);
+                if (g2) c0_accum(nacc, bin0, R2);
+                if (g3) c0_accum(nacc, bin0, R3);
+            }
+            __syncthreads();
+
+            if (t < 128) {
+                int v = bin0 + t;
+                float deg = nacc[768 + t];
+                float S0 = nacc[t],       S1 = nacc[128 + t], S2 = nacc[256 + t];
+                float S3 = nacc[384 + t], S4 = nacc[512 + t], S5 = nacc[640 + t];
+                float inv = 1.f / fmaxf(deg, 1.f);
+                float xv = A.x0[v];
+                #pragma unroll
+                for (int o = 0; o < 12; o++) {
+                    float msg = wsm[60 + o] * S0 + wsm[o] * S1 + wsm[12 + o] * S2 +
+                                wsm[24 + o] * S3 + wsm[36 + o] * S4 + wsm[48 + o] * S5;
+                    A.y[v * 12 + o] = msg * inv + xv * wsm[72 + o] + wsm[84 + o];
+                }
+            }
+            break;
+        }
+        B -= NB0;
+        if (B < NB1) {
+            int* hist = iSP;
+            int* cur  = iSP + 32;
+            int b = B;
+            int lo = A.bs1[b], hi = A.bs1[b + 1];
+            int bin0 = b << 5;
+            if (t < 32) hist[t] = 0;
+            __syncthreads();
+            const float* payw = (const float*)A.pay1;
+            for (int j0 = lo + t; j0 < hi; j0 += 512) {
+                unsigned k0 = __float_as_uint(payw[4 * j0]);
+                int j1 = j0 + 256;
+                bool g1 = j1 < hi;
+                unsigned k1 = g1 ? __float_as_uint(payw[4 * j1]) : 0u;
+                atomicAdd(&hist[(int)(k0 >> 16) - bin0], 1);
+                if (g1) atomicAdd(&hist[(int)(k1 >> 16) - bin0], 1);
+            }
+            __syncthreads();
+            if (t < 32) {
+                int v = hist[t];
+                int val = v;
+                #pragma unroll
+                for (int d = 1; d < 32; d <<= 1) {
+                    int u = __shfl_up(val, d);
+                    if (t >= d) val += u;
+                }
+                cur[t] = lo + val - v;
+                A.rp1[bin0 + t] = lo + val - v;
+                if (b == NB1 - 1 && t == 31) A.rp1[NB1 * 32] = hi;
+            }
+            __syncthreads();
+            for (int j0 = lo + t; j0 < hi; j0 += 512) {
+                float4 R0 = A.pay1[j0];
+                int j1 = j0 + 256;
+                bool g1 = j1 < hi;
+                float4 R1;
+                if (g1) R1 = A.pay1[j1];
+                int rel0 = (int)(__float_as_uint(R0.x) >> 16) - bin0;
+                int p0 = atomicAdd(&cur[rel0], 1);
+                A.rec1[p0] = R0;
+                if (g1) {
+                    int rel1 = (int)(__float_as_uint(R1.x) >> 16) - bin0;
+                    int p1 = atomicAdd(&cur[rel1], 1);
+                    A.rec1[p1] = R1;
+                }
+            }
+            break;
+        }
+        B -= NB1;
+        if (B < 5) {
+            if (t < 64) {
+                const WArgs& wa = A.wa;
+                int l = B;
+                const float* w2l = wa.w2[l];
+                const float* b2l = wa.b2[l];
+                int cico = wa.cico[l];
+                float d[21];
+                #pragma unroll
+                for (int i = 0; i < 21; i++) d[i] = 0.f;
+                for (int u = t; u < cico; u += 64) {
+                    float b = b2l[u];
+                    float w[5];
+                    #pragma unroll
+                    for (int k = 0; k < 5; k++) w[k] = w2l[k * cico + u];
+                    int p = 0;
+                    #pragma unroll
+                    for (int k = 0; k < 5; k++) {
+                        #pragma unroll
+                        for (int k2 = k; k2 < 5; k2++) d[p++] += w[k] * w[k2];
+                    }
+                    #pragma unroll
+                    for (int k = 0; k < 5; k++) d[15 + k] += b * w[k];
+                    d[20] += b * b;
+                }
+                #pragma unroll
+                for (int i = 0; i < 21; i++) {
+                    #pragma unroll
+                    for (int off = 32; off; off >>= 1) d[i] += __shfl_down(d[i], off);
+                }
+                if (t == 0) {
+                    const float* H1 = wa.H + l * 20;
+                    const float* H2 = H1 + 5;
+                    float sq = (float)wa.E[l] * d[20];
+                    #pragma unroll
+                    for (int k = 0; k < 5; k++) sq += 2.f * d[15 + k] * H1[k];
+                    int p = 0;
+                    #pragma unroll
+                    for (int k = 0; k < 5; k++) {
+                        #pragma unroll
+                        for (int k2 = k; k2 < 5; k2++) {
+                            sq += ((k == k2) ? 1.f : 2.f) * d[p] * H2[p];
+                            p++;
+                        }
+                    }
+                    wa.sq[l] = sq;
+                }
+            }
+            break;
+        }
+        B -= 5;
+        {
+            const SegArgs& a = A.sa;
+            int sg = 0;
+            while (sg < 9 && B >= a.tstart[sg + 1]) sg++;
+            int i0 = (B - a.tstart[sg]) * 1024;
+            const int* idx = a.idx[sg];
+            int* cnt = a.cnt[sg];
+            const int* rp = a.rp[sg];
+            int* out = a.out[sg];
+            int n = a.n[sg];
+            #pragma unroll
+            for (int j = 0; j < 4; j++) {
+                int i = i0 + j * 256 + t;
+                if (i < n) {
+                    int d = idx[i];
+                    int p = atomicSub(&cnt[d], 1) - 1;
+                    out[rp[d] + p] = i;
+                }
+            }
+        }
+        break;
+    }
+
+    case 6:
+        pool_body<12>(16384, A.crp[0], A.cnid[0], A.y, A.pos0,
+                      A.xn[0], A.pn[0], vb * 256 + t);
+        break;
+    case 7:
+        conv1s_body(A, vb, t, SP, iSP);
+        break;
+    case 8:
+        pool_body<20>(4096, A.crp[1], A.cnid[1], A.y, A.pn[0],
+                      A.xn[1], A.pn[1], vb * 256 + t);
+        break;
+    case 9:
+        coop_body<23, 28>(A, 2, vb, t, SP, iSP);
+        break;
+    case 10:
+        pool_body<28>(1024, A.crp[2], A.cnid[2], A.y, A.pn[1],
+                      A.xn[2], A.pn[2], vb * 256 + t);
+        break;
+    case 11:
+        coop_body<31, 36>(A, 3, vb, t, SP, iSP);
+        break;
+    case 12:
+        pool_body<36>(256, A.crp[3], A.cnid[3], A.y, A.pn[2],
+                      A.xn[3], A.pn[3], vb * 256 + t);
+        break;
+    case 13:
+        coop_body<39, 44>(A, 4, vb, t, SP, iSP);
+        break;
+    case 14:
+        pool_body<44>(64, A.crp[4], A.cnid[4], A.y, A.pn[3],
+                      A.xn[4], A.pn[4], vb * 256 + t);
+        break;
+
+    case 15: {
+        float* logit = SP;
+        float* roff  = SP + 80;
+        const float* x5 = A.xn[4];
+        if (t < 80) {
+            int b = t / 10, j = t % 10;
+            float acc = A.fc_b[j];
+            for (int k = 0; k < 376; k++)
+                acc += x5[b * 376 + k] * A.fc_w[k * 10 + j];
+            logit[t] = acc;
+        }
+        __syncthreads();
+        if (t < 8) {
+            float m = -1e30f;
+            for (int j = 0; j < 10; j++) m = fmaxf(m, logit[t * 10 + j]);
+            float ssum = 0.f;
+            for (int j = 0; j < 10; j++) ssum += expf(logit[t * 10 + j] - m);
+            roff[t] = m + logf(ssum);
+        }
+        __syncthreads();
+        if (t < 80) A.out[t] = logit[t] - roff[t / 10];
+        if (t == 0) {
+            const float* sq = A.wa.sq;
+            float closs = 0.f;
+            closs += sq[0] * (1.0f / 12582912.0f);
+            closs += sq[1] * (1.0f / 78643200.0f);
+            closs += sq[2] * (1.0f / 42205184.0f);
+            closs += sq[3] * (1.0f / 18284544.0f);
+            closs += sq[4] * (1.0f / 7028736.0f);
+            A.out[80] = closs;
+        }
+        break;
+    }
+    }
+}
+
+__global__ __launch_bounds__(256, 4) void mega_k(MegaArgs A)
+{
+    __shared__ alignas(16) float SP[2560];
+    cg::grid_group grid = cg::this_grid();
+    const int t = threadIdx.x;
+    const int G = gridDim.x;
+
+    for (int s = 1; s <= 15; s++) {
+        for (int vb = blockIdx.x; vb < A.W[s]; vb += G) {
+            run_stage(A, s, vb, t, SP);
+            __syncthreads();
+        }
+        grid.sync();
+    }
+}
+
+__global__ __launch_bounds__(256, 4) void stage_k(MegaArgs A, int s)
+{
+    __shared__ alignas(16) float SP[2560];
+    run_stage(A, s, blockIdx.x, threadIdx.x, SP);
 }
 
 
@@ -806,10 +883,7 @@
     size_t sqO  = alw(8);
     size_t xnO[5], pnO[5];
     for (int l = 0; l < 5; l++) xnO[l] = alw((size_t)NSa[l + 1] * (COa[l] + 3));
-    for (int l = 0; l < 5; l++) pnO[l] = alw((size_t)NSa[l] * 3 / 4 + 64);
     for (int l = 0; l < 5; l++) pnO[l] = alw((size_t)NSa[l + 1] * 3);
-
-    hipMemsetAsync(d_ws, 0, zeroWords * 4, stream);
 
     SegArgs sa{};
     int nseg = 0;
@@ -852,13 +926,10 @@
     sx.tilesum = wsw + tsO;
     sx.tileoff = wsw + toO;
 
-    float4* pay2 = (float4*)(wsw + payO);
-    float4* pay1 = (float4*)(wsw + pay1O);
-    float4* rec1 = (float4*)(wsw + rec1O);
-    float*  Hp   = (float*)(wsw + HO);
+    float*  Hp = (float*)(wsw + HO);
 
     HArgs ha{};
-    int bs = 0;
+    int hsB = 0;
     ha.bstart[0] = 0;
     ha.eattr[0] = (const float*)d_in[4];
     ha.w1[0] = (const float*)d_in[6];
@@ -869,10 +940,10 @@
         ha.w1[l]    = (const float*)d_in[6 + 10 * l];
         ha.b1[l]    = (const float*)d_in[7 + 10 * l];
         ha.E[l]     = ESa[l];
-        ha.bstart[l] = bs;
-        bs += (ESa[l] + 2047) / 2048;
-    }
-    ha.bstart[5] = bs;
+        ha.bstart[l] = hsB;
+        hsB += (ESa[l] + 2047) / 2048;
+    }
+    ha.bstart[5] = hsB;
     ha.H = Hp;
 
     WArgs wa{};
@@ -885,67 +956,72 @@
     wa.H  = Hp;
     wa.sq = (float*)(wsw + sqO);
 
-    countA_k<<<TILES0 + TILES1 + bs + tiles, 256, 0, stream>>>(
-        sa, ha, (const int*)d_in[3], (const int*)d_in[13],
-        wsw + MO, wsw + M1O, bs);
-    scanP1_k<<<NB0 + NB1 + btiles, 256, 0, stream>>>(
-        sa, sx, wsw + MO, wsw + M2O, wsw + ctO,
-        wsw + M1O, wsw + M21O, wsw + ct1O);
-    scanP2_k<<<3, 512, 0, stream>>>(sa, sx, wsw + ctO, wsw + bsO,
-                                    wsw + ct1O, wsw + bs1O);
-    scanP3_k<<<TILES0 + TILES1 + btiles, 256, 0, stream>>>(
-        sa, sx,
-        (const int*)d_in[2], (const int*)d_in[3], (const float*)d_in[4],
-        x0, wsw + M2O, wsw + bsO, pay2,
-        (const float*)d_in[6], (const float*)d_in[7], Hp,
-        (const int*)d_in[12], (const int*)d_in[13], (const float*)d_in[14],
-        wsw + M21O, wsw + bs1O, pay1);
-
-    float* yb = (float*)(wsw + yO);
-
-    scatC_k<<<NB0 + NB1 + 5 + tiles, 256, 0, stream>>>(
-        sa, wa, pay2, wsw + bsO,
-        (const float*)d_in[8], (const float*)d_in[9],
-        (const float*)d_in[10], (const float*)d_in[11], x0, yb,
-        pay1, wsw + bs1O, wsw + rpO[1], rec1);
-
-    pool_k<12><<<(NSa[1] * 15 + 255) / 256, 256, 0, stream>>>(
-        NSa[1], wsw + crpO[0], wsw + cnidO[0], yb, pos0,
-        (float*)(wsw + xnO[0]), (float*)(wsw + pnO[0]));
-
-    conv1s_k<<<NSa[1], 256, 0, stream>>>(
-        wsw + rpO[1], rec1,
-        (const float*)d_in[16], (const float*)d_in[17],
-        (const float*)d_in[18], (const float*)d_in[19],
-        (const float*)d_in[20], (const float*)d_in[21],
-        (const float*)(wsw + xnO[0]), yb);
-    pool_k<20><<<(NSa[2] * 23 + 255) / 256, 256, 0, stream>>>(
-        NSa[2], wsw + crpO[1], wsw + cnidO[1], yb,
-        (const float*)(wsw + pnO[0]),
-        (float*)(wsw + xnO[1]), (float*)(wsw + pnO[1]));
-
-#define LVLC(l, CI_, CO_) do {                                                 \
-    const float* xin   = (const float*)(wsw + xnO[(l) - 1]);                   \
-    const float* posin = (const float*)(wsw + pnO[(l) - 1]);                   \
-    int N = NSa[(l)], NN = NSa[(l) + 1];                                       \
-    coop_conv_k<CI_, CO_><<<N, 256, 0, stream>>>(                              \
-        wsw + rpO[(l)], wsw + eidO[(l)],                                       \
-        (const int*)d_in[2 + 10 * (l)], (const float*)d_in[4 + 10 * (l)],      \
-        (const float*)d_in[6 + 10 * (l)], (const float*)d_in[7 + 10 * (l)],    \
-        (const float*)d_in[8 + 10 * (l)], (const float*)d_in[9 + 10 * (l)],    \
-        (const float*)d_in[10 + 10 * (l)], (const float*)d_in[11 + 10 * (l)],  \
-        xin, yb);                                                              \
-    pool_k<CO_><<<(NN * ((CO_) + 3) + 255) / 256, 256, 0, stream>>>(           \
-        NN, wsw + crpO[(l)], wsw + cnidO[(l)], yb, posin,                      \
-        (float*)(wsw + xnO[(l)]), (float*)(wsw + pnO[(l)]));                   \
-} while (0)
-
-    LVLC(2, 23, 28);
-    LVLC(3, 31, 36);
-    LVLC(4, 39, 44);
-#undef LVLC
-
-    fc_k<<<1, 128, 0, stream>>>((const float*)(wsw + xnO[4]),
-                                (const float*)d_in[52], (const float*)d_in[53],
-                                wa.sq, (float*)d_out);
+    MegaArgs A{};
+    A.sa = sa; A.sx = sx; A.ha = ha; A.wa = wa;
+    A.src0 = (const int*)d_in[2];  A.dst0 = (const int*)d_in[3];
+    A.ea0  = (const float*)d_in[4];
+    A.src1 = (const int*)d_in[12]; A.dst1 = (const int*)d_in[13];
+    A.ea1  = (const float*)d_in[14];
+    A.x0 = x0; A.pos0 = pos0;
+    A.M = wsw + MO; A.M2 = wsw + M2O; A.colTotal = wsw + ctO;
+    A.bucketStart = wsw + bsO;
+    A.M1 = wsw + M1O; A.M21 = wsw + M21O; A.ct1 = wsw + ct1O; A.bs1 = wsw + bs1O;
+    A.pay2 = (float4*)(wsw + payO);
+    A.pay1 = (float4*)(wsw + pay1O);
+    A.rec1 = (float4*)(wsw + rec1O);
+    A.rp1  = wsw + rpO[1];
+    for (int l = 0; l < 5; l++) {
+        A.w1[l]   = (const float*)d_in[6 + 10 * l];
+        A.b1[l]   = (const float*)d_in[7 + 10 * l];
+        A.w2[l]   = (const float*)d_in[8 + 10 * l];
+        A.b2[l]   = (const float*)d_in[9 + 10 * l];
+        A.root[l] = (const float*)d_in[10 + 10 * l];
+        A.bias[l] = (const float*)d_in[11 + 10 * l];
+        A.srcL[l] = (const int*)d_in[2 + 10 * l];
+        A.eaL[l]  = (const float*)d_in[4 + 10 * l];
+        A.crp[l]  = wsw + crpO[l];
+        A.cnid[l] = wsw + cnidO[l];
+        A.xn[l]   = (float*)(wsw + xnO[l]);
+        A.pn[l]   = (float*)(wsw + pnO[l]);
+    }
+    for (int l = 2; l < 5; l++) {
+        A.rp[l]  = wsw + rpO[l];
+        A.eid[l] = wsw + eidO[l];
+    }
+    A.y = (float*)(wsw + yO);
+    A.fc_w = (const float*)d_in[52];
+    A.fc_b = (const float*)d_in[53];
+    A.out = (float*)d_out;
+    A.hsB = hsB;
+
+    A.W[1]  = TILES0 + TILES1 + hsB + tiles;
+    A.W[2]  = NB0 + NB1 + btiles;
+    A.W[3]  = 3;
+    A.W[4]  = TILES0 + TILES1 + btiles;
+    A.W[5]  = NB0 + NB1 + 5 + tiles;
+    A.W[6]  = (NSa[1] * 15 + 255) / 256;
+    A.W[7]  = NSa[1];
+    A.W[8]  = (NSa[2] * 23 + 255) / 256;
+    A.W[9]  = NSa[2];
+    A.W[10] = (NSa[3] * 31 + 255) / 256;
+    A.W[11] = NSa[3];
+    A.W[12] = (NSa[4] * 39 + 255) / 256;
+    A.W[13] = NSa[4];
+    A.W[14] = (NSa[5] * 47 + 255) / 256;
+    A.W[15] = 1;
+
+    hipMemsetAsync(d_ws, 0, zeroWords * 4, stream);
+
+    static int coopOK = -1;
+    hipError_t err = hipErrorUnknown;
+    if (coopOK != 0) {
+        void* kargs[] = { (void*)&A };
+        err = hipLaunchCooperativeKernel((const void*)mega_k, dim3(1024), dim3(256),
+                                         kargs, 0, stream);
+        if (coopOK < 0) coopOK = (err == hipSuccess) ? 1 : 0;
+    }
+    if (coopOK == 0) {
+        for (int s = 1; s <= 15; s++)
+            stage_k<<<dim3(A.W[s]), dim3(256), 0, stream>>>(A, s);
+    }
 }
```

New measurement: 421.8 us. +4.5%, slower.
